# Kernel tuning notes

Hardware: AMD Instinct MI355X
Metric: run time of the kernel (lower is better)

## Reference

```python
import jax, jax.numpy as jnp
import numpy as np

D, H, DFF, NE, ND, B = 512, 8, 2048, 64, 64, 16

def _ln(x, g, b):
    m = x.mean(-1, keepdims=True)
    v = ((x - m) ** 2).mean(-1, keepdims=True)
    return (x - m) * jax.lax.rsqrt(v + 1e-5) * g + b

def _mha(q, k, v, Wi, bi, Wo, bo, h=H):
    # q,k,v: (L, B, d) seq-first, like torch nn.MultiheadAttention (eval mode)
    Lq, Bb, d = q.shape
    hd = d // h
    Wq, Wk, Wv = jnp.split(Wi, 3, axis=0)
    bq, bk, bv = jnp.split(bi, 3)
    def proj(x, W, bb):
        y = x @ W.T + bb                                  # (L, B, d)
        return y.reshape(x.shape[0], Bb, h, hd).transpose(1, 2, 0, 3)  # (B, h, L, hd)
    qh = proj(q, Wq, bq) * (hd ** -0.5)
    kh = proj(k, Wk, bk)
    vh = proj(v, Wv, bv)
    a = jax.nn.softmax(jnp.einsum('bhqe,bhke->bhqk', qh, kh), axis=-1)
    o = jnp.einsum('bhqk,bhke->bhqe', a, vh).transpose(2, 0, 1, 3).reshape(Lq, Bb, d)
    return o @ Wo.T + bo

def _ffn(x, W1, b1, W2, b2):
    return jax.nn.relu(x @ W1.T + b1) @ W2.T + b2

def _forward(enc, dec, ec_Wi, ec_bi, ec_Wo, ec_bo, dc_Wi, dc_bi, dc_Wo, dc_bo,
             es_Wi, es_bi, es_Wo, es_bo, ds_Wi, ds_bi, ds_Wo, ds_bo,
             eff_W1, eff_b1, eff_W2, eff_b2, dff_W1, dff_b1, dff_W2, dff_b2,
             n_ec_g, n_ec_b, n_es_g, n_es_b, n_ef_g, n_ef_b, n_dc_g, n_dc_b,
             n_dci_g, n_dci_b, n_ds_g, n_ds_b, n_df_g, n_df_b, pW, pWb, pv, pb):
    f_n = _ln(enc, n_ec_g, n_ec_b)   # (ne, B, d) -- normed once, reused for all j
    G_n = _ln(dec, n_dc_g, n_dc_b)   # (nd, B, d)
    # dec_cross for all j at once (key/value is the single token f_j)
    dc_out = jax.vmap(lambda fj: _mha(G_n, fj[None], fj[None], dc_Wi, dc_bi, dc_Wo, dc_bo))(f_n)  # (ne, nd, B, d)
    G_fj = dec[None] + dc_out                            # (ne, nd, B, d)
    G_im = _ln(G_fj, n_dci_g, n_dci_b)
    # enc_cross for all j at once (query is the single token f_j)
    ec_out = jax.vmap(lambda fj, Gj: _mha(fj[None], Gj, Gj, ec_Wi, ec_bi, ec_Wo, ec_bo)[0])(f_n, G_im)  # (ne, B, d)
    enc1 = enc + ec_out
    # attention pooling over the ne fusion copies
    G_c = G_fj.transpose(2, 1, 0, 3)                     # (B, nd, ne, d)
    energy = jnp.tanh(G_c @ pW.T + pWb + pb)
    w = jax.nn.softmax(energy @ pv.T, axis=2)            # (B, nd, ne, 1)
    dec1 = (G_c * w).sum(axis=2).transpose(1, 0, 2)      # (nd, B, d)
    # self-attention + FFN (pre-norm residual)
    en = _ln(enc1, n_es_g, n_es_b)
    enc2 = enc1 + _mha(en, en, en, es_Wi, es_bi, es_Wo, es_bo)
    dn = _ln(dec1, n_ds_g, n_ds_b)
    dec2 = dec1 + _mha(dn, dn, dn, ds_Wi, ds_bi, ds_Wo, ds_bo)
    enc3 = enc2 + _ffn(_ln(enc2, n_ef_g, n_ef_b), eff_W1, eff_b1, eff_W2, eff_b2)
    dec3 = dec2 + _ffn(_ln(dec2, n_df_g, n_df_b), dff_W1, dff_b1, dff_W2, dff_b2)
    return (enc3, dec3)

def setup_inputs() -> dict:
    key = jax.random.key(0)
    ks = iter(jax.random.split(key, 64))
    def w(shape, scale=0.05):
        return jax.random.normal(next(ks), shape, jnp.float32) * scale
    d, dff = D, DFF
    inp = {
        'enc': jax.random.normal(next(ks), (NE, B, d), jnp.float32),
        'dec': jax.random.normal(next(ks), (ND, B, d), jnp.float32),
    }
    for p in ['ec', 'dc', 'es', 'ds']:
        inp[p + '_Wi'] = w((3 * d, d)); inp[p + '_bi'] = jnp.zeros(3 * d, jnp.float32)
        inp[p + '_Wo'] = w((d, d)); inp[p + '_bo'] = jnp.zeros(d, jnp.float32)
    for p in ['eff', 'dff']:
        inp[p + '_W1'] = w((dff, d)); inp[p + '_b1'] = jnp.zeros(dff, jnp.float32)
        inp[p + '_W2'] = w((d, dff)); inp[p + '_b2'] = jnp.zeros(d, jnp.float32)
    for p in ['n_ec', 'n_es', 'n_ef', 'n_dc', 'n_dci', 'n_ds', 'n_df']:
        inp[p + '_g'] = jnp.ones(d, jnp.float32); inp[p + '_b'] = jnp.zeros(d, jnp.float32)
    inp['pW'] = w((d, d)); inp['pWb'] = jnp.zeros(d, jnp.float32)
    inp['pv'] = w((1, d)); inp['pb'] = jnp.zeros(d, jnp.float32)
    return inp

def reference(enc, dec, ec_Wi, ec_bi, ec_Wo, ec_bo, dc_Wi, dc_bi, dc_Wo, dc_bo,
              es_Wi, es_bi, es_Wo, es_bo, ds_Wi, ds_bi, ds_Wo, ds_bo,
              eff_W1, eff_b1, eff_W2, eff_b2, dff_W1, dff_b1, dff_W2, dff_b2,
              n_ec_g, n_ec_b, n_es_g, n_es_b, n_ef_g, n_ef_b, n_dc_g, n_dc_b,
              n_dci_g, n_dci_b, n_ds_g, n_ds_b, n_df_g, n_df_b, pW, pWb, pv, pb):
    return _forward(enc, dec, ec_Wi, ec_bi, ec_Wo, ec_bo, dc_Wi, dc_bi, dc_Wo, dc_bo,
                    es_Wi, es_bi, es_Wo, es_bo, ds_Wi, ds_bi, ds_Wo, ds_bo,
                    eff_W1, eff_b1, eff_W2, eff_b2, dff_W1, dff_b1, dff_W2, dff_b2,
                    n_ec_g, n_ec_b, n_es_g, n_es_b, n_ef_g, n_ef_b, n_dc_g, n_dc_b,
                    n_dci_g, n_dci_b, n_ds_g, n_ds_b, n_df_g, n_df_b, pW, pWb, pv, pb)
```

## Files before the change

kernel.cpp:

```cpp
#include <hip/hip_runtime.h>


typedef __bf16 bf16_t;
typedef bf16_t bf16x8 __attribute__((ext_vector_type(8)));
typedef float f32x4 __attribute__((ext_vector_type(4)));
typedef unsigned short u16x4 __attribute__((ext_vector_type(4)));
typedef unsigned short u16x8 __attribute__((ext_vector_type(8)));

__device__ inline unsigned short f2bf(float f) {
  unsigned int u = __float_as_uint(f);
  u += 0x7fffu + ((u >> 16) & 1u);
  return (unsigned short)(u >> 16);
}
__device__ inline float bf2f(unsigned short u) {
  return __uint_as_float(((unsigned int)u) << 16);
}

__device__ inline float wsum(float v) {
#pragma unroll
  for (int o = 1; o < 64; o <<= 1) v += __shfl_xor(v, o);
  return v;
}
__device__ inline float wmax(float v) {
#pragma unroll
  for (int o = 1; o < 64; o <<= 1) v = fmaxf(v, __shfl_xor(v, o));
  return v;
}

struct CastJob {
  const float* src;
  unsigned short* dst;
  int n;
  const float* cs;
};
struct CastBatch {
  CastJob j[15];
};

__global__ __launch_bounds__(256) void cast_w(CastBatch cb) {
  const CastJob jb = cb.j[blockIdx.y];
  const int stride = 32 * 256 * 4;
  for (int i = (blockIdx.x * 256 + threadIdx.x) * 4; i < jb.n; i += stride) {
    float4 v = *(const float4*)(jb.src + i);
    if (jb.cs) {
      int k = i & 511;
      v.x *= jb.cs[k];
      v.y *= jb.cs[k + 1];
      v.z *= jb.cs[k + 2];
      v.w *= jb.cs[k + 3];
    }
    u16x4 o = {f2bf(v.x), f2bf(v.y), f2bf(v.z), f2bf(v.w)};
    *(u16x4*)(jb.dst + i) = o;
  }
}

__device__ inline void ln_body(const float* __restrict__ x,
                               const float* __restrict__ g,
                               const float* __restrict__ be,
                               unsigned short* __restrict__ y, int t) {
  float v0 = x[t], v1 = x[t + 256];
  float s = wsum(v0 + v1);
  float s2 = wsum(v0 * v0 + v1 * v1);
  __shared__ float sh[8];
  int w = t >> 6, lane = t & 63;
  if (lane == 0) { sh[w] = s; sh[4 + w] = s2; }
  __syncthreads();
  s = sh[0] + sh[1] + sh[2] + sh[3];
  s2 = sh[4] + sh[5] + sh[6] + sh[7];
  float mean = s * (1.f / 512.f);
  float var = s2 * (1.f / 512.f) - mean * mean;
  float r = rsqrtf(var + 1e-5f);
  y[t] = f2bf((v0 - mean) * r * g[t] + be[t]);
  y[t + 256] = f2bf((v1 - mean) * r * g[t + 256] + be[t + 256]);
}

__device__ inline void stats_body(const float* __restrict__ x,
                                  float* __restrict__ m, float* __restrict__ q2,
                                  unsigned short* __restrict__ xb, int t,
                                  int row) {
  float v0 = x[t], v1 = x[t + 256];
  if (xb) {
    xb[t] = f2bf(v0);
    xb[t + 256] = f2bf(v1);
  }
  float s = wsum(v0 + v1);
  float s2 = wsum(v0 * v0 + v1 * v1);
  __shared__ float sh2[8];
  int w = t >> 6, lane = t & 63;
  if (lane == 0) { sh2[w] = s; sh2[4 + w] = s2; }
  __syncthreads();
  if (t == 0) {
    s = sh2[0] + sh2[1] + sh2[2] + sh2[3];
    s2 = sh2[4] + sh2[5] + sh2[6] + sh2[7];
    m[row] = s * (1.f / 512.f);
    q2[row] = s2 * (1.f / 512.f);
  }
}

__global__ __launch_bounds__(256) void ln_stats_kernel(
    const float* __restrict__ enc, const float* __restrict__ g,
    const float* __restrict__ be, unsigned short* __restrict__ f_n,
    const float* __restrict__ dec, float* __restrict__ md,
    float* __restrict__ q2d, unsigned short* __restrict__ dec_b) {
  int row = blockIdx.x;
  if (row < 1024) {
    ln_body(enc + (size_t)row * 512, g, be, f_n + (size_t)row * 512,
            threadIdx.x);
  } else {
    row -= 1024;
    stats_body(dec + (size_t)row * 512, md, q2d, dec_b + (size_t)row * 512,
               threadIdx.x, row);
  }
}

__global__ __launch_bounds__(256) void stats_kernel(
    const float* __restrict__ X, float* __restrict__ m, float* __restrict__ q2,
    unsigned short* __restrict__ Xb) {
  int row = blockIdx.x;
  stats_body(X + (size_t)row * 512, m, q2,
             Xb ? Xb + (size_t)row * 512 : nullptr, threadIdx.x, row);
}

__global__ __launch_bounds__(256) void ln2_kernel(
    const float* __restrict__ X0, const float* __restrict__ g0,
    const float* __restrict__ b0, unsigned short* __restrict__ Y0,
    const float* __restrict__ X1, const float* __restrict__ g1,
    const float* __restrict__ b1, unsigned short* __restrict__ Y1) {
  int row = blockIdx.x;
  if (row < 1024) {
    ln_body(X0 + (size_t)row * 512, g0, b0, Y0 + (size_t)row * 512, threadIdx.x);
  } else {
    row -= 1024;
    ln_body(X1 + (size_t)row * 512, g1, b1, Y1 + (size_t)row * 512, threadIdx.x);
  }
}

__global__ __launch_bounds__(256) void uvec_kernel(
    const float* __restrict__ Wk, const float* __restrict__ Wv,
    const float* __restrict__ bk, const float* __restrict__ bv,
    const float* __restrict__ g, const float* __restrict__ beta,
    float* __restrict__ u_k, float* __restrict__ u_v,
    float* __restrict__ c_k, float* __restrict__ c_v) {
  int n = blockIdx.x * 4 + (threadIdx.x >> 6);
  int lane = threadIdx.x & 63;
  const float* wk = Wk + (size_t)n * 512;
  const float* wv = Wv + (size_t)n * 512;
  float uk = 0.f, uv = 0.f, ck = 0.f, cv = 0.f;
#pragma unroll
  for (int k0 = 0; k0 < 512; k0 += 64) {
    int k = k0 + lane;
    float a = wk[k], b2 = wv[k], gg = g[k], bb = beta[k];
    uk += a * gg;
    ck += a * bb;
    uv += b2 * gg;
    cv += b2 * bb;
  }
  uk = wsum(uk);
  uv = wsum(uv);
  ck = wsum(ck);
  cv = wsum(cv);
  if (lane == 0) {
    u_k[n] = uk;
    u_v[n] = uv;
    c_k[n] = ck + bk[n];
    c_v[n] = cv + bv[n];
  }
}

__global__ __launch_bounds__(256) void mr_kernel(
    const unsigned short* __restrict__ decb, const unsigned short* __restrict__ tbb,
    const float* __restrict__ md, const float* __restrict__ q2d,
    const float* __restrict__ mt, const float* __restrict__ q2t,
    float* __restrict__ mArr, float* __restrict__ rArr) {
  int wid = blockIdx.x * 4 + (threadIdx.x >> 6);
  int lane = threadIdx.x & 63;
  int b = wid & 15;
  int i = (wid >> 4) & 63;
  int j = wid >> 10;
  const unsigned short* dr = decb + (size_t)(i * 16 + b) * 512 + lane * 8;
  const unsigned short* tr = tbb + (size_t)(j * 16 + b) * 512 + lane * 8;
  u16x8 a = *(const u16x8*)dr;
  u16x8 c = *(const u16x8*)tr;
  float s = 0.f;
#pragma unroll
  for (int k = 0; k < 8; ++k) s += bf2f(a[k]) * bf2f(c[k]);
  s = wsum(s);
  if (lane == 0) {
    float mean = md[i * 16 + b] + mt[j * 16 + b];
    float msq = q2d[i * 16 + b] + q2t[j * 16 + b] + 2.f * s * (1.f / 512.f);
    float var = msq - mean * mean;
    int idx = b * 4096 + j * 64 + i;
    mArr[idx] = mean;
    rArr[idx] = rsqrtf(var + 1e-5f);
  }
}

__global__ __launch_bounds__(256) void ec_attn(
    const unsigned short* __restrict__ Qe, const unsigned short* __restrict__ Kd,
    const unsigned short* __restrict__ Kt, const unsigned short* __restrict__ Vd,
    const unsigned short* __restrict__ Vt, const float* __restrict__ u_k,
    const float* __restrict__ u_v, const float* __restrict__ c_k,
    const float* __restrict__ c_v, const float* __restrict__ mArr,
    const float* __restrict__ rArr, unsigned short* __restrict__ O) {
  int h = blockIdx.x & 7;
  int b = blockIdx.x >> 3;
  __shared__ unsigned short Qs[64][72];
  __shared__ unsigned short Ks[64][72];
  __shared__ unsigned short VdT[64][72];
  __shared__ unsigned short Ps[64][72];
  __shared__ float ms[64][66];
  __shared__ float rs[64][66];
  __shared__ float stp[64][4], sup[64][4], scp[64][4];
  __shared__ float stv[64], suv[64], scv[64], swv[64], swmv[64];
  int t = threadIdx.x;
  {
    int row = t >> 2;
    int qt = t & 3;
    int cb = qt * 16;
    size_t base = (size_t)(row * 16 + b) * 512 + h * 64 + cb;
    u16x8 q0 = *(const u16x8*)(Qe + base);
    u16x8 q1 = *(const u16x8*)(Qe + base + 8);
    u16x8 k0 = *(const u16x8*)(Kd + base);
    u16x8 k1 = *(const u16x8*)(Kd + base + 8);
    u16x8 kt0 = *(const u16x8*)(Kt + base);
    u16x8 kt1 = *(const u16x8*)(Kt + base + 8);
    u16x8 v0 = *(const u16x8*)(Vd + base);
    u16x8 v1 = *(const u16x8*)(Vd + base + 8);
    *(u16x8*)&Qs[row][cb] = q0;
    *(u16x8*)&Qs[row][cb + 8] = q1;
    *(u16x8*)&Ks[row][cb] = k0;
    *(u16x8*)&Ks[row][cb + 8] = k1;
#pragma unroll
    for (int jj = 0; jj < 8; ++jj) VdT[cb + jj][row] = v0[jj];
#pragma unroll
    for (int jj = 0; jj < 8; ++jj) VdT[cb + 8 + jj][row] = v1[jj];
    float st_ = 0.f, su_ = 0.f, sc_ = 0.f;
#pragma unroll
    for (int jj = 0; jj < 8; ++jj) {
      float qa = bf2f(q0[jj]), qb = bf2f(q1[jj]);
      st_ += qa * bf2f(kt0[jj]) + qb * bf2f(kt1[jj]);
      su_ += qa * u_k[h * 64 + cb + jj] + qb * u_k[h * 64 + cb + 8 + jj];
      sc_ += qa * c_k[h * 64 + cb + jj] + qb * c_k[h * 64 + cb + 8 + jj];
    }
    stp[row][qt] = st_;
    sup[row][qt] = su_;
    scp[row][qt] = sc_;
  }
#pragma unroll
  for (int k = 0; k < 16; ++k) {
    int idx = t + k * 256;
    ms[idx >> 6][idx & 63] = mArr[(size_t)b * 4096 + idx];
    rs[idx >> 6][idx & 63] = rArr[(size_t)b * 4096 + idx];
  }
  __syncthreads();
  if (t < 64) {
    stv[t] = stp[t][0] + stp[t][1] + stp[t][2] + stp[t][3];
    suv[t] = sup[t][0] + sup[t][1] + sup[t][2] + sup[t][3];
    scv[t] = scp[t][0] + scp[t][1] + scp[t][2] + scp[t][3];
  }
  __syncthreads();
  int wave = t >> 6, lane = t & 63;
  int fr = lane & 15, fg = lane >> 4;
  f32x4 sacc[4] = {};
  bf16x8 aq0 = *(const bf16x8*)&Qs[wave * 16 + fr][fg * 8];
  bf16x8 aq1 = *(const bf16x8*)&Qs[wave * 16 + fr][32 + fg * 8];
#pragma unroll
  for (int nt = 0; nt < 4; ++nt) {
    bf16x8 b0 = *(const bf16x8*)&Ks[nt * 16 + fr][fg * 8];
    bf16x8 b1 = *(const bf16x8*)&Ks[nt * 16 + fr][32 + fg * 8];
    sacc[nt] = __builtin_amdgcn_mfma_f32_16x16x32_bf16(aq0, b0, sacc[nt], 0, 0, 0);
    sacc[nt] = __builtin_amdgcn_mfma_f32_16x16x32_bf16(aq1, b1, sacc[nt], 0, 0, 0);
  }
#pragma unroll
  for (int r = 0; r < 4; ++r) {
    int j = wave * 16 + fg * 4 + r;
    float stj = stv[j], suj = suv[j], scj = scv[j];
    float a0, a1, a2, a3;
    {
      int i0 = fr, i1 = 16 + fr, i2 = 32 + fr, i3 = 48 + fr;
      a0 = rs[j][i0] * (sacc[0][r] + stj - ms[j][i0] * suj) + scj;
      a1 = rs[j][i1] * (sacc[1][r] + stj - ms[j][i1] * suj) + scj;
      a2 = rs[j][i2] * (sacc[2][r] + stj - ms[j][i2] * suj) + scj;
      a3 = rs[j][i3] * (sacc[3][r] + stj - ms[j][i3] * suj) + scj;
    }
    float mx = fmaxf(fmaxf(a0, a1), fmaxf(a2, a3));
#pragma unroll
    for (int o = 1; o < 16; o <<= 1) mx = fmaxf(mx, __shfl_xor(mx, o));
    a0 = __expf(a0 - mx);
    a1 = __expf(a1 - mx);
    a2 = __expf(a2 - mx);
    a3 = __expf(a3 - mx);
    float se = a0 + a1 + a2 + a3;
#pragma unroll
    for (int o = 1; o < 16; o <<= 1) se += __shfl_xor(se, o);
    float inv = 1.f / se;
    float w0 = a0 * inv * rs[j][fr];
    float w1 = a1 * inv * rs[j][16 + fr];
    float w2 = a2 * inv * rs[j][32 + fr];
    float w3 = a3 * inv * rs[j][48 + fr];
    float sw = w0 + w1 + w2 + w3;
    float swm = w0 * ms[j][fr] + w1 * ms[j][16 + fr] + w2 * ms[j][32 + fr] +
                w3 * ms[j][48 + fr];
#pragma unroll
    for (int o = 1; o < 16; o <<= 1) {
      sw += __shfl_xor(sw, o);
      swm += __shfl_xor(swm, o);
    }
    Ps[j][fr] = f2bf(w0);
    Ps[j][16 + fr] = f2bf(w1);
    Ps[j][32 + fr] = f2bf(w2);
    Ps[j][48 + fr] = f2bf(w3);
    if (fr == 0) {
      swv[j] = sw;
      swmv[j] = swm;
    }
  }
  f32x4 oc[4] = {};
  bf16x8 ap0 = *(const bf16x8*)&Ps[wave * 16 + fr][fg * 8];
  bf16x8 ap1 = *(const bf16x8*)&Ps[wave * 16 + fr][32 + fg * 8];
#pragma unroll
  for (int nt = 0; nt < 4; ++nt) {
    bf16x8 b0 = *(const bf16x8*)&VdT[nt * 16 + fr][fg * 8];
    bf16x8 b1 = *(const bf16x8*)&VdT[nt * 16 + fr][32 + fg * 8];
    oc[nt] = __builtin_amdgcn_mfma_f32_16x16x32_bf16(ap0, b0, oc[nt], 0, 0, 0);
    oc[nt] = __builtin_amdgcn_mfma_f32_16x16x32_bf16(ap1, b1, oc[nt], 0, 0, 0);
  }
#pragma unroll
  for (int nt = 0; nt < 4; ++nt) {
    int d = nt * 16 + fr;
    float uvd = u_v[h * 64 + d];
    float cvd = c_v[h * 64 + d];
#pragma unroll
    for (int r = 0; r < 4; ++r) {
      int j = wave * 16 + fg * 4 + r;
      size_t gidx = (size_t)(j * 16 + b) * 512 + h * 64 + d;
      float o = oc[nt][r] + swv[j] * bf2f(Vt[gidx]) - swmv[j] * uvd + cvd;
      O[gidx] = f2bf(o);
    }
  }
}

__global__ __launch_bounds__(256) void pool_kernel(
    const float* __restrict__ Ed, const float* __restrict__ Et,
    const float* __restrict__ pv, const float* __restrict__ dec,
    const unsigned short* __restrict__ tbf, float* __restrict__ dec1) {
  int i = blockIdx.x;
  int b = blockIdx.y;
  int t = threadIdx.x;
  int wave = t >> 6, lane = t & 63;
  float edv[8], pvv[8];
  const float* ed = Ed + (size_t)(i * 16 + b) * 512;
#pragma unroll
  for (int c = 0; c < 8; ++c) {
    edv[c] = ed[c * 64 + lane];
    pvv[c] = pv[c * 64 + lane];
  }
  __shared__ float esh[64];
  __shared__ float wsh[64];
#pragma unroll 1
  for (int jl = 0; jl < 16; ++jl) {
    int j = wave * 16 + jl;
    const float* et = Et + (size_t)(j * 16 + b) * 512;
    float s = 0.f;
#pragma unroll
    for (int c = 0; c < 8; ++c) {
      float x = edv[c] + et[c * 64 + lane];
      float e2 = __expf(2.f * x);
      float th = 1.f - 2.f * __builtin_amdgcn_rcpf(e2 + 1.f);
      s += th * pvv[c];
    }
    s = wsum(s);
    if (lane == 0) esh[j] = s;
  }
  __syncthreads();
  if (t < 64) {
    float e = esh[t];
    float mx = wmax(e);
    float ex = __expf(e - mx);
    float se = wsum(ex);
    wsh[t] = ex / se;
  }
  __syncthreads();
  size_t rowib = (size_t)(i * 16 + b) * 512;
  int d2 = t * 2;
  float2 dv = *(const float2*)(dec + rowib + d2);
  float acc0 = dv.x, acc1 = dv.y;
#pragma unroll 8
  for (int j2 = 0; j2 < 64; ++j2) {
    const unsigned short* tp = tbf + (size_t)(j2 * 16 + b) * 512 + d2;
    float w = wsh[j2];
    acc0 += w * bf2f(tp[0]);
    acc1 += w * bf2f(tp[1]);
  }
  float2 ov = {acc0, acc1};
  *(float2*)(dec1 + rowib + d2) = ov;
}

__global__ __launch_bounds__(256) void self_attn(
    const unsigned short* __restrict__ QKVe, unsigned short* __restrict__ Oe,
    const unsigned short* __restrict__ QKVd, unsigned short* __restrict__ Od) {
  const unsigned short* QKV = blockIdx.y ? QKVd : QKVe;
  unsigned short* O = blockIdx.y ? Od : Oe;
  int h = blockIdx.x & 7;
  int b = blockIdx.x >> 3;
  __shared__ unsigned short Qs[64][72];
  __shared__ unsigned short Ksh[64][72];
  __shared__ unsigned short VT[64][72];
  __shared__ unsigned short Ps[64][72];
  int t = threadIdx.x;
  {
    int row = t >> 2;
    int cb = (t & 3) * 16;
    const unsigned short* src =
        QKV + (size_t)(row * 16 + b) * 1536 + h * 64 + cb;
    u16x8 q0 = *(const u16x8*)(src);
    u16x8 q1 = *(const u16x8*)(src + 8);
    u16x8 k0 = *(const u16x8*)(src + 512);
    u16x8 k1 = *(const u16x8*)(src + 520);
    u16x8 v0 = *(const u16x8*)(src + 1024);
    u16x8 v1 = *(const u16x8*)(src + 1032);
    *(u16x8*)&Qs[row][cb] = q0;
    *(u16x8*)&Qs[row][cb + 8] = q1;
    *(u16x8*)&Ksh[row][cb] = k0;
    *(u16x8*)&Ksh[row][cb + 8] = k1;
#pragma unroll
    for (int jj = 0; jj < 8; ++jj) VT[cb + jj][row] = v0[jj];
#pragma unroll
    for (int jj = 0; jj < 8; ++jj) VT[cb + 8 + jj][row] = v1[jj];
  }
  __syncthreads();
  int wave = t >> 6, lane = t & 63;
  int fr = lane & 15, fg = lane >> 4;
  f32x4 sc[4] = {};
  bf16x8 aq0 = *(const bf16x8*)&Qs[wave * 16 + fr][fg * 8];
  bf16x8 aq1 = *(const bf16x8*)&Qs[wave * 16 + fr][32 + fg * 8];
#pragma unroll
  for (int nt = 0; nt < 4; ++nt) {
    bf16x8 b0 = *(const bf16x8*)&Ksh[nt * 16 + fr][fg * 8];
    bf16x8 b1 = *(const bf16x8*)&Ksh[nt * 16 + fr][32 + fg * 8];
    sc[nt] = __builtin_amdgcn_mfma_f32_16x16x32_bf16(aq0, b0, sc[nt], 0, 0, 0);
    sc[nt] = __builtin_amdgcn_mfma_f32_16x16x32_bf16(aq1, b1, sc[nt], 0, 0, 0);
  }
#pragma unroll
  for (int r = 0; r < 4; ++r) {
    float a0 = sc[0][r] * 0.125f, a1 = sc[1][r] * 0.125f;
    float a2 = sc[2][r] * 0.125f, a3 = sc[3][r] * 0.125f;
    float mx = fmaxf(fmaxf(a0, a1), fmaxf(a2, a3));
#pragma unroll
    for (int o = 1; o < 16; o <<= 1) mx = fmaxf(mx, __shfl_xor(mx, o));
    a0 = __expf(a0 - mx);
    a1 = __expf(a1 - mx);
    a2 = __expf(a2 - mx);
    a3 = __expf(a3 - mx);
    float se = a0 + a1 + a2 + a3;
#pragma unroll
    for (int o = 1; o < 16; o <<= 1) se += __shfl_xor(se, o);
    float inv = 1.f / se;
    int prow = wave * 16 + fg * 4 + r;
    Ps[prow][0 + fr] = f2bf(a0 * inv);
    Ps[prow][16 + fr] = f2bf(a1 * inv);
    Ps[prow][32 + fr] = f2bf(a2 * inv);
    Ps[prow][48 + fr] = f2bf(a3 * inv);
  }
  f32x4 oc[4] = {};
  bf16x8 ap0 = *(const bf16x8*)&Ps[wave * 16 + fr][fg * 8];
  bf16x8 ap1 = *(const bf16x8*)&Ps[wave * 16 + fr][32 + fg * 8];
#pragma unroll
  for (int nt = 0; nt < 4; ++nt) {
    bf16x8 b0 = *(const bf16x8*)&VT[nt * 16 + fr][fg * 8];
    bf16x8 b1 = *(const bf16x8*)&VT[nt * 16 + fr][32 + fg * 8];
    oc[nt] = __builtin_amdgcn_mfma_f32_16x16x32_bf16(ap0, b0, oc[nt], 0, 0, 0);
    oc[nt] = __builtin_amdgcn_mfma_f32_16x16x32_bf16(ap1, b1, oc[nt], 0, 0, 0);
  }
#pragma unroll
  for (int nt = 0; nt < 4; ++nt) {
#pragma unroll
    for (int r = 0; r < 4; ++r) {
      int q = wave * 16 + fg * 4 + r;
      int d = nt * 16 + fr;
      O[(size_t)(q * 16 + b) * 512 + h * 64 + d] = f2bf(oc[nt][r]);
    }
  }
}

struct GemmJob {
  const unsigned short* X;
  const unsigned short* W;
  const float* bias;
  const float* resid;
  float* Y;
  unsigned short* Ybf;
  float scale;
  int relu;
};
struct GemmBatch {
  GemmJob j[5];
};

__global__ __launch_bounds__(256) void gemm_bf16(GemmBatch gb, int M, int N,
                                                 int K) {
  const GemmJob jb = gb.j[blockIdx.z];
  __shared__ unsigned short As[64][72];
  __shared__ unsigned short Bs[64][72];
  const int t = threadIdx.x;
  const int lane = t & 63;
  const int wave = t >> 6;
  const int wr = wave >> 1;
  const int wc = wave & 1;
  const int bm = blockIdx.y * 64;
  const int bn = blockIdx.x * 64;

  f32x4 acc[2][2] = {};
  const unsigned short* Xp = jb.X + (size_t)bm * K;
  const unsigned short* Wp = jb.W + (size_t)bn * K;

  const int c0 = t, c1 = t + 256;
  const int r0 = c0 >> 3, o0 = (c0 & 7) * 8;
  const int r1 = c1 >> 3, o1 = (c1 & 7) * 8;

  u16x8 xa0 = *(const u16x8*)&Xp[(size_t)r0 * K + o0];
  u16x8 xa1 = *(const u16x8*)&Xp[(size_t)r1 * K + o1];
  u16x8 wa0 = *(const u16x8*)&Wp[(size_t)r0 * K + o0];
  u16x8 wa1 = *(const u16x8*)&Wp[(size_t)r1 * K + o1];

  for (int k0 = 0; k0 < K; k0 += 64) {
    *(u16x8*)&As[r0][o0] = xa0;
    *(u16x8*)&As[r1][o1] = xa1;
    *(u16x8*)&Bs[r0][o0] = wa0;
    *(u16x8*)&Bs[r1][o1] = wa1;
    __syncthreads();
    if (k0 + 64 < K) {
      int kn = k0 + 64;
      xa0 = *(const u16x8*)&Xp[(size_t)r0 * K + kn + o0];
      xa1 = *(const u16x8*)&Xp[(size_t)r1 * K + kn + o1];
      wa0 = *(const u16x8*)&Wp[(size_t)r0 * K + kn + o0];
      wa1 = *(const u16x8*)&Wp[(size_t)r1 * K + kn + o1];
    }
#pragma unroll
    for (int ks = 0; ks < 2; ++ks) {
      int kk = ks * 32 + (lane >> 4) * 8;
      int fr = lane & 15;
      bf16x8 a0 = *(const bf16x8*)&As[wr * 32 + fr][kk];
      bf16x8 a1 = *(const bf16x8*)&As[wr * 32 + 16 + fr][kk];
      bf16x8 b0 = *(const bf16x8*)&Bs[wc * 32 + fr][kk];
      bf16x8 b1 = *(const bf16x8*)&Bs[wc * 32 + 16 + fr][kk];
      acc[0][0] = __builtin_amdgcn_mfma_f32_16x16x32_bf16(a0, b0, acc[0][0], 0, 0, 0);
      acc[0][1] = __builtin_amdgcn_mfma_f32_16x16x32_bf16(a0, b1, acc[0][1], 0, 0, 0);
      acc[1][0] = __builtin_amdgcn_mfma_f32_16x16x32_bf16(a1, b0, acc[1][0], 0, 0, 0);
      acc[1][1] = __builtin_amdgcn_mfma_f32_16x16x32_bf16(a1, b1, acc[1][1], 0, 0, 0);
    }
    __syncthreads();
  }
#pragma unroll
  for (int mt = 0; mt < 2; ++mt) {
#pragma unroll
    for (int nt = 0; nt < 2; ++nt) {
      int col = bn + wc * 32 + nt * 16 + (lane & 15);
      int rowb = bm + wr * 32 + mt * 16 + (lane >> 4) * 4;
      float bia = jb.bias ? jb.bias[col] : 0.f;
#pragma unroll
      for (int r = 0; r < 4; ++r) {
        float v = (acc[mt][nt][r] + bia) * jb.scale;
        if (jb.relu) v = fmaxf(v, 0.f);
        if (jb.resid) v += jb.resid[(size_t)(rowb + r) * N + col];
        size_t idx = (size_t)(rowb + r) * N + col;
        if (jb.Y) jb.Y[idx] = v;
        if (jb.Ybf) jb.Ybf[idx] = f2bf(v);
      }
    }
  }
}

extern "C" void kernel_launch(void* const* d_in, const int* in_sizes, int n_in,
                              void* d_out, int out_size, void* d_ws,
                              size_t ws_size, hipStream_t stream) {
  const float* enc = (const float*)d_in[0];
  const float* dec = (const float*)d_in[1];
  const float* ec_Wi = (const float*)d_in[2];
  const float* ec_bi = (const float*)d_in[3];
  const float* ec_Wo = (const float*)d_in[4];
  const float* ec_bo = (const float*)d_in[5];
  const float* dc_Wi = (const float*)d_in[6];
  const float* dc_bi = (const float*)d_in[7];
  const float* dc_Wo = (const float*)d_in[8];
  const float* dc_bo = (const float*)d_in[9];
  const float* es_Wi = (const float*)d_in[10];
  const float* es_bi = (const float*)d_in[11];
  const float* es_Wo = (const float*)d_in[12];
  const float* es_bo = (const float*)d_in[13];
  const float* ds_Wi = (const float*)d_in[14];
  const float* ds_bi = (const float*)d_in[15];
  const float* ds_Wo = (const float*)d_in[16];
  const float* ds_bo = (const float*)d_in[17];
  const float* eff_W1 = (const float*)d_in[18];
  const float* eff_b1 = (const float*)d_in[19];
  const float* eff_W2 = (const float*)d_in[20];
  const float* eff_b2 = (const float*)d_in[21];
  const float* dff_W1 = (const float*)d_in[22];
  const float* dff_b1 = (const float*)d_in[23];
  const float* dff_W2 = (const float*)d_in[24];
  const float* dff_b2 = (const float*)d_in[25];
  const float* n_ec_g = (const float*)d_in[26];
  const float* n_ec_b = (const float*)d_in[27];
  const float* n_es_g = (const float*)d_in[28];
  const float* n_es_b = (const float*)d_in[29];
  const float* n_ef_g = (const float*)d_in[30];
  const float* n_ef_b = (const float*)d_in[31];
  const float* n_dci_g = (const float*)d_in[34];
  const float* n_dci_b = (const float*)d_in[35];
  const float* n_ds_g = (const float*)d_in[36];
  const float* n_ds_b = (const float*)d_in[37];
  const float* n_df_g = (const float*)d_in[38];
  const float* n_df_b = (const float*)d_in[39];
  const float* pW = (const float*)d_in[40];
  const float* pWb = (const float*)d_in[41];
  const float* pv = (const float*)d_in[42];
  const float* pb = (const float*)d_in[43];

  float* ws = (float*)d_ws;
  const size_t U = 524288;
  float* Ed = ws + 3 * U;
  float* tb = ws + 4 * U;
  float* Et = ws + 7 * U;
  float* enc1 = ws + 8 * U;
  float* dec1 = ws + 9 * U;
  float* enc2 = ws + 10 * U;
  float* dec2 = ws + 11 * U;
  float* sm = ws + 12 * U;
  float* md = sm;
  float* q2d = sm + 1024;
  float* mt = sm + 2048;
  float* q2t = sm + 3072;
  float* u_k = sm + 4096;
  float* u_v = sm + 4608;
  float* c_k = sm + 5120;
  float* c_v = sm + 5632;
  float* mArr = sm + 6144;
  float* rArr = sm + 6144 + 65536;
  unsigned short* ub0 = (unsigned short*)ws;
  unsigned short* Qe_b = ub0 + 0 * U;
  unsigned short* Kd_b = ub0 + 1 * U;
  unsigned short* Vd_b = ub0 + 2 * U;
  unsigned short* Kt_b = ub0 + 3 * U;
  unsigned short* Vt_b = ub0 + 4 * U;
  unsigned short* ub = (unsigned short*)(ws + 12 * U + 137216);
  const int W262 = 262144, W786 = 786432, W1M = 1048576;
  unsigned short* w_dcWv = ub;
  unsigned short* w_ecWq = w_dcWv + W262;
  unsigned short* w_ecWkg = w_ecWq + W262;
  unsigned short* w_ecWvg = w_ecWkg + W262;
  unsigned short* w_pW = w_ecWvg + W262;
  unsigned short* w_dcWo = w_pW + W262;
  unsigned short* w_ecWo = w_dcWo + W262;
  unsigned short* w_esWi = w_ecWo + W262;
  unsigned short* w_dsWi = w_esWi + W786;
  unsigned short* w_esWo = w_dsWi + W786;
  unsigned short* w_dsWo = w_esWo + W262;
  unsigned short* w_effW1 = w_dsWo + W262;
  unsigned short* w_dffW1 = w_effW1 + W1M;
  unsigned short* w_effW2 = w_dffW1 + W1M;
  unsigned short* w_dffW2 = w_effW2 + W1M;
  unsigned short* actb = w_dffW2 + W1M;
  unsigned short* f_n_b = actb;
  unsigned short* V1_b = actb + U;
  unsigned short* dec_b = actb + 2 * U;
  unsigned short* tb_b = actb + 3 * U;
  unsigned short* Oec_b = actb + 4 * U;
  unsigned short* nbE = f_n_b;
  unsigned short* nbD = V1_b;
  unsigned short* OaE = dec_b;
  unsigned short* OaD = tb_b;
  unsigned short* QKVe_b = (unsigned short*)(ws + 0 * U);
  unsigned short* QKVd_b = (unsigned short*)(ws + 2 * U);
  unsigned short* He_b = (unsigned short*)(ws + 0 * U);
  unsigned short* Hd_b = (unsigned short*)(ws + 2 * U);

  const float* dc_Wv = dc_Wi + 1024 * 512;
  const float* dc_bv = dc_bi + 1024;
  const float* ec_Wq = ec_Wi;
  const float* ec_bq = ec_bi;
  const float* ec_Wk = ec_Wi + 512 * 512;
  const float* ec_bk = ec_bi + 512;
  const float* ec_Wv = ec_Wi + 1024 * 512;
  const float* ec_bv = ec_bi + 1024;

  {
    CastBatch cb{};
    cb.j[0] = {dc_Wv, w_dcWv, W262, nullptr};
    cb.j[1] = {ec_Wq, w_ecWq, W262, nullptr};
    cb.j[2] = {ec_Wk, w_ecWkg, W262, n_dci_g};
    cb.j[3] = {ec_Wv, w_ecWvg, W262, n_dci_g};
    cb.j[4] = {pW, w_pW, W262, nullptr};
    cb.j[5] = {dc_Wo, w_dcWo, W262, nullptr};
    cb.j[6] = {ec_Wo, w_ecWo, W262, nullptr};
    cb.j[7] = {es_Wi, w_esWi, W786, nullptr};
    cb.j[8] = {ds_Wi, w_dsWi, W786, nullptr};
    cb.j[9] = {es_Wo, w_esWo, W262, nullptr};
    cb.j[10] = {ds_Wo, w_dsWo, W262, nullptr};
    cb.j[11] = {eff_W1, w_effW1, W1M, nullptr};
    cb.j[12] = {dff_W1, w_dffW1, W1M, nullptr};
    cb.j[13] = {eff_W2, w_effW2, W1M, nullptr};
    cb.j[14] = {dff_W2, w_dffW2, W1M, nullptr};
    cast_w<<<dim3(32, 15), 256, 0, stream>>>(cb);
  }
  ln_stats_kernel<<<2048, 256, 0, stream>>>(enc, n_ec_g, n_ec_b, f_n_b, dec,
                                            md, q2d, dec_b);
  uvec_kernel<<<128, 256, 0, stream>>>(ec_Wk, ec_Wv, ec_bk, ec_bv, n_dci_g,
                                       n_dci_b, u_k, u_v, c_k, c_v);
  {
    GemmBatch gb{};
    gb.j[0] = {f_n_b, w_dcWv, dc_bv, nullptr, nullptr, V1_b, 1.f, 0};
    gb.j[1] = {f_n_b, w_ecWq, ec_bq, nullptr, nullptr, Qe_b, 0.125f, 0};
    gb.j[2] = {dec_b, w_ecWkg, nullptr, nullptr, nullptr, Kd_b, 1.f, 0};
    gb.j[3] = {dec_b, w_ecWvg, nullptr, nullptr, nullptr, Vd_b, 1.f, 0};
    gb.j[4] = {dec_b, w_pW, pWb, nullptr, Ed, nullptr, 1.f, 0};
    gemm_bf16<<<dim3(8, 16, 5), 256, 0, stream>>>(gb, 1024, 512, 512);
  }
  {
    GemmBatch gb{};
    gb.j[0] = {V1_b, w_dcWo, dc_bo, nullptr, tb, tb_b, 1.f, 0};
    gemm_bf16<<<dim3(8, 16, 1), 256, 0, stream>>>(gb, 1024, 512, 512);
  }
  stats_kernel<<<1024, 256, 0, stream>>>(tb, mt, q2t, nullptr);
  {
    GemmBatch gb{};
    gb.j[0] = {tb_b, w_ecWkg, nullptr, nullptr, nullptr, Kt_b, 1.f, 0};
    gb.j[1] = {tb_b, w_ecWvg, nullptr, nullptr, nullptr, Vt_b, 1.f, 0};
    gb.j[2] = {tb_b, w_pW, pb, nullptr, Et, nullptr, 1.f, 0};
    gemm_bf16<<<dim3(8, 16, 3), 256, 0, stream>>>(gb, 1024, 512, 512);
  }
  mr_kernel<<<16384, 256, 0, stream>>>(dec_b, tb_b, md, q2d, mt, q2t, mArr,
                                       rArr);
  ec_attn<<<128, 256, 0, stream>>>(Qe_b, Kd_b, Kt_b, Vd_b, Vt_b, u_k, u_v, c_k,
                                   c_v, mArr, rArr, Oec_b);
  pool_kernel<<<dim3(64, 16), 256, 0, stream>>>(Ed, Et, pv, dec, tb_b, dec1);
  {
    GemmBatch gb{};
    gb.j[0] = {Oec_b, w_ecWo, ec_bo, enc, enc1, nullptr, 1.f, 0};
    gemm_bf16<<<dim3(8, 16, 1), 256, 0, stream>>>(gb, 1024, 512, 512);
  }
  ln2_kernel<<<2048, 256, 0, stream>>>(enc1, n_es_g, n_es_b, nbE, dec1, n_ds_g,
                                       n_ds_b, nbD);
  {
    GemmBatch gb{};
    gb.j[0] = {nbE, w_esWi, es_bi, nullptr, nullptr, QKVe_b, 1.f, 0};
    gb.j[1] = {nbD, w_dsWi, ds_bi, nullptr, nullptr, QKVd_b, 1.f, 0};
    gemm_bf16<<<dim3(24, 16, 2), 256, 0, stream>>>(gb, 1024, 1536, 512);
  }
  self_attn<<<dim3(128, 2), 256, 0, stream>>>(QKVe_b, OaE, QKVd_b, OaD);
  {
    GemmBatch gb{};
    gb.j[0] = {OaE, w_esWo, es_bo, enc1, enc2, nullptr, 1.f, 0};
    gb.j[1] = {OaD, w_dsWo, ds_bo, dec1, dec2, nullptr, 1.f, 0};
    gemm_bf16<<<dim3(8, 16, 2), 256, 0, stream>>>(gb, 1024, 512, 512);
  }
  ln2_kernel<<<2048, 256, 0, stream>>>(enc2, n_ef_g, n_ef_b, nbE, dec2, n_df_g,
                                       n_df_b, nbD);
  {
    GemmBatch gb{};
    gb.j[0] = {nbE, w_effW1, eff_b1, nullptr, nullptr, He_b, 1.f, 1};
    gb.j[1] = {nbD, w_dffW1, dff_b1, nullptr, nullptr, Hd_b, 1.f, 1};
    gemm_bf16<<<dim3(32, 16, 2), 256, 0, stream>>>(gb, 1024, 2048, 512);
  }
  float* out = (float*)d_out;
  {
    GemmBatch gb{};
    gb.j[0] = {He_b, w_effW2, eff_b2, enc2, out, nullptr, 1.f, 0};
    gb.j[1] = {Hd_b, w_dffW2, dff_b2, dec2, out + U, nullptr, 1.f, 0};
    gemm_bf16<<<dim3(8, 16, 2), 256, 0, stream>>>(gb, 1024, 512, 2048);
  }
}
```

Before: 317.8 us.

## Fuse LayerNorms into GEMMs, merge casts/stats/uvec and mr into fewer launches

Removes the standalone LayerNorm, stats, uvec, mr and cast kernels. GEMM epilogues now accumulate per-row sum and sum-of-squares with atomics, and the following GEMM applies LayerNorm while loading its fp32 input tile. Weight casts are spread between a merged phase0 kernel and an extra z-slice of the first GEMM. The mr dot products run as an MFMA slice of another GEMM, and ec_attn and pool are merged into one attnpool kernel that also produces dec1 stats. This cuts launch count and intermediate traffic, but adds atomics, per-tile recomputation of normalization, and variance computed as E[x^2]-mean^2.

Result: slower. 339.8 us (+6.9%).

```diff
diff --git a/kernel.cpp b/kernel.cpp
--- a/kernel.cpp
+++ b/kernel.cpp
@@ -33,26 +33,6 @@
   int n;
   const float* cs;
 };
-struct CastBatch {
-  CastJob j[15];
-};
-
-__global__ __launch_bounds__(256) void cast_w(CastBatch cb) {
-  const CastJob jb = cb.j[blockIdx.y];
-  const int stride = 32 * 256 * 4;
-  for (int i = (blockIdx.x * 256 + threadIdx.x) * 4; i < jb.n; i += stride) {
-    float4 v = *(const float4*)(jb.src + i);
-    if (jb.cs) {
-      int k = i & 511;
-      v.x *= jb.cs[k];
-      v.y *= jb.cs[k + 1];
-      v.z *= jb.cs[k + 2];
-      v.w *= jb.cs[k + 3];
-    }
-    u16x4 o = {f2bf(v.x), f2bf(v.y), f2bf(v.z), f2bf(v.w)};
-    *(u16x4*)(jb.dst + i) = o;
-  }
-}
 
 __device__ inline void ln_body(const float* __restrict__ x,
                                const float* __restrict__ g,
@@ -97,113 +77,327 @@
   }
 }
 
-__global__ __launch_bounds__(256) void ln_stats_kernel(
-    const float* __restrict__ enc, const float* __restrict__ g,
-    const float* __restrict__ be, unsigned short* __restrict__ f_n,
-    const float* __restrict__ dec, float* __restrict__ md,
-    float* __restrict__ q2d, unsigned short* __restrict__ dec_b) {
-  int row = blockIdx.x;
-  if (row < 1024) {
-    ln_body(enc + (size_t)row * 512, g, be, f_n + (size_t)row * 512,
-            threadIdx.x);
+struct Phase0Args {
+  const float* enc; const float* g_ec; const float* b_ec; unsigned short* f_n;
+  const float* dec; float* md; float* q2d; unsigned short* dec_b;
+  CastJob cast[6];
+  const float* Wk; const float* Wv; const float* bk; const float* bv;
+  const float* g_dci; const float* b_dci;
+  float* u_k; float* u_v; float* c_k; float* c_v;
+  float* zbase; int zcount;
+};
+
+__global__ __launch_bounds__(256) void phase0(Phase0Args a) {
+  int bx = blockIdx.x;
+  const int t = threadIdx.x;
+  if (bx < 2048) {
+    int row = bx;
+    if (row < 1024) {
+      ln_body(a.enc + (size_t)row * 512, a.g_ec, a.b_ec,
+              a.f_n + (size_t)row * 512, t);
+    } else {
+      row -= 1024;
+      stats_body(a.dec + (size_t)row * 512, a.md, a.q2d,
+                 a.dec_b + (size_t)row * 512, t, row);
+    }
+    return;
+  }
+  bx -= 2048;
+  if (bx < 256) {
+    const int total = 6 * 262144;
+    const int stride = 256 * 256 * 4;
+    for (int e = (bx * 256 + t) * 4; e < total; e += stride) {
+      int jj = e >> 18;
+      int i = e & 262143;
+      const CastJob cj = a.cast[jj];
+      float4 v = *(const float4*)(cj.src + i);
+      if (cj.cs) {
+        int k = i & 511;
+        v.x *= cj.cs[k]; v.y *= cj.cs[k + 1];
+        v.z *= cj.cs[k + 2]; v.w *= cj.cs[k + 3];
+      }
+      u16x4 o = {f2bf(v.x), f2bf(v.y), f2bf(v.z), f2bf(v.w)};
+      *(u16x4*)(cj.dst + i) = o;
+    }
+    return;
+  }
+  bx -= 256;
+  if (bx < 128) {
+    int n = bx * 4 + (t >> 6);
+    int lane = t & 63;
+    const float* wk = a.Wk + (size_t)n * 512;
+    const float* wv = a.Wv + (size_t)n * 512;
+    float uk = 0.f, uv = 0.f, ck = 0.f, cv = 0.f;
+#pragma unroll
+    for (int k0 = 0; k0 < 512; k0 += 64) {
+      int k = k0 + lane;
+      float x = wk[k], y = wv[k], gg = a.g_dci[k], bb = a.b_dci[k];
+      uk += x * gg; ck += x * bb;
+      uv += y * gg; cv += y * bb;
+    }
+    uk = wsum(uk); uv = wsum(uv); ck = wsum(ck); cv = wsum(cv);
+    if (lane == 0) {
+      a.u_k[n] = uk; a.u_v[n] = uv;
+      a.c_k[n] = ck + a.bk[n]; a.c_v[n] = cv + a.bv[n];
+    }
+    return;
+  }
+  for (int i = t; i < a.zcount; i += 256) a.zbase[i] = 0.f;
+}
+
+struct GemmJob {
+  const unsigned short* X;
+  const float* Xf;
+  const float* Asum; const float* Asq;
+  const float* g; const float* be;
+  const unsigned short* W;
+  const float* bias;
+  const float* resid;
+  float* Y;
+  unsigned short* Ybf;
+  float* Ssum; float* Ssq;
+  float scale;
+  int relu;
+};
+struct MrJob {
+  const unsigned short* A; const unsigned short* B;
+  const float* md; const float* q2d;
+  const float* ts; const float* tsq;
+  float* mArr; float* rArr;
+};
+struct GemmBatch {
+  GemmJob j[5];
+  MrJob mr;
+  CastJob c[9];
+};
+
+__device__ inline u16x8 fold_pack(float4 va, float4 vb, const float* gp,
+                                  const float* bp, float m, float ri) {
+  float4 g0 = *(const float4*)gp;
+  float4 g1 = *(const float4*)(gp + 4);
+  float4 e0 = *(const float4*)bp;
+  float4 e1 = *(const float4*)(bp + 4);
+  u16x8 o;
+  o[0] = f2bf((va.x - m) * ri * g0.x + e0.x);
+  o[1] = f2bf((va.y - m) * ri * g0.y + e0.y);
+  o[2] = f2bf((va.z - m) * ri * g0.z + e0.z);
+  o[3] = f2bf((va.w - m) * ri * g0.w + e0.w);
+  o[4] = f2bf((vb.x - m) * ri * g1.x + e1.x);
+  o[5] = f2bf((vb.y - m) * ri * g1.y + e1.y);
+  o[6] = f2bf((vb.z - m) * ri * g1.z + e1.z);
+  o[7] = f2bf((vb.w - m) * ri * g1.w + e1.w);
+  return o;
+}
+
+__global__ __launch_bounds__(256) void gemm_bf16(GemmBatch gb, int M, int N,
+                                                 int K, int cast_z, int mr_z) {
+  const int t = threadIdx.x;
+  if ((int)blockIdx.z == cast_z) {
+    const int nb = gridDim.x * gridDim.y;
+    const int bid = blockIdx.y * gridDim.x + blockIdx.x;
+    const int stride = nb * 256 * 4;
+#pragma unroll 1
+    for (int jj = 0; jj < 9; ++jj) {
+      const CastJob cj = gb.c[jj];
+      if (!cj.src) continue;
+      for (int i = (bid * 256 + t) * 4; i < cj.n; i += stride) {
+        float4 v = *(const float4*)(cj.src + i);
+        u16x4 o = {f2bf(v.x), f2bf(v.y), f2bf(v.z), f2bf(v.w)};
+        *(u16x4*)(cj.dst + i) = o;
+      }
+    }
+    return;
+  }
+  __shared__ unsigned short As[64][72];
+  __shared__ unsigned short Bs[64][72];
+  const int lane = t & 63;
+  const int wave = t >> 6;
+  const int wr = wave >> 1;
+  const int wc = wave & 1;
+  const int fr = lane & 15;
+  const int fg = lane >> 4;
+  const int c1 = t + 256;
+  const int r0 = t >> 3, o0 = (t & 7) * 8;
+  const int r1 = c1 >> 3, o1 = (c1 & 7) * 8;
+
+  if ((int)blockIdx.z == mr_z) {
+    const int bb = blockIdx.y * gridDim.x + blockIdx.x;
+    if (bb >= 16) return;
+    const unsigned short* Ap = gb.mr.A + (size_t)bb * 512;
+    const unsigned short* Bp = gb.mr.B + (size_t)bb * 512;
+    f32x4 acc[2][2] = {};
+    for (int k0 = 0; k0 < 512; k0 += 64) {
+      *(u16x8*)&As[r0][o0] = *(const u16x8*)&Ap[(size_t)r0 * 8192 + k0 + o0];
+      *(u16x8*)&As[r1][o1] = *(const u16x8*)&Ap[(size_t)r1 * 8192 + k0 + o1];
+      *(u16x8*)&Bs[r0][o0] = *(const u16x8*)&Bp[(size_t)r0 * 8192 + k0 + o0];
+      *(u16x8*)&Bs[r1][o1] = *(const u16x8*)&Bp[(size_t)r1 * 8192 + k0 + o1];
+      __syncthreads();
+#pragma unroll
+      for (int ks = 0; ks < 2; ++ks) {
+        int kk = ks * 32 + fg * 8;
+        bf16x8 a0 = *(const bf16x8*)&As[wr * 32 + fr][kk];
+        bf16x8 a1 = *(const bf16x8*)&As[wr * 32 + 16 + fr][kk];
+        bf16x8 b0 = *(const bf16x8*)&Bs[wc * 32 + fr][kk];
+        bf16x8 b1 = *(const bf16x8*)&Bs[wc * 32 + 16 + fr][kk];
+        acc[0][0] = __builtin_amdgcn_mfma_f32_16x16x32_bf16(a0, b0, acc[0][0], 0, 0, 0);
+        acc[0][1] = __builtin_amdgcn_mfma_f32_16x16x32_bf16(a0, b1, acc[0][1], 0, 0, 0);
+        acc[1][0] = __builtin_amdgcn_mfma_f32_16x16x32_bf16(a1, b0, acc[1][0], 0, 0, 0);
+        acc[1][1] = __builtin_amdgcn_mfma_f32_16x16x32_bf16(a1, b1, acc[1][1], 0, 0, 0);
+      }
+      __syncthreads();
+    }
+#pragma unroll
+    for (int nt = 0; nt < 2; ++nt) {
+      int j = wc * 32 + nt * 16 + fr;
+      float mtv = gb.mr.ts[j * 16 + bb] * (1.f / 512.f);
+      float qtv = gb.mr.tsq[j * 16 + bb] * (1.f / 512.f);
+#pragma unroll
+      for (int mt = 0; mt < 2; ++mt) {
+        int ibase = wr * 32 + mt * 16 + fg * 4;
+#pragma unroll
+        for (int r = 0; r < 4; ++r) {
+          int i = ibase + r;
+          float s = acc[mt][nt][r];
+          float mean = gb.mr.md[i * 16 + bb] + mtv;
+          float msq = gb.mr.q2d[i * 16 + bb] + qtv + s * (2.f / 512.f);
+          int idx = bb * 4096 + j * 64 + i;
+          gb.mr.mArr[idx] = mean;
+          gb.mr.rArr[idx] = rsqrtf(msq - mean * mean + 1e-5f);
+        }
+      }
+    }
+    return;
+  }
+
+  const GemmJob jb = gb.j[blockIdx.z];
+  const int bm = blockIdx.y * 64;
+  const int bn = blockIdx.x * 64;
+  const bool fold = jb.Xf != nullptr;
+  f32x4 acc[2][2] = {};
+  const unsigned short* Wp = jb.W + (size_t)bn * K;
+  const unsigned short* Xp = jb.X ? jb.X + (size_t)bm * K : nullptr;
+
+  float lm0 = 0.f, lr0i = 0.f, lm1 = 0.f, lr1i = 0.f;
+  if (fold) {
+    float s = jb.Asum[bm + r0], q = jb.Asq[bm + r0];
+    lm0 = s * (1.f / 512.f);
+    lr0i = rsqrtf(q * (1.f / 512.f) - lm0 * lm0 + 1e-5f);
+    s = jb.Asum[bm + r1]; q = jb.Asq[bm + r1];
+    lm1 = s * (1.f / 512.f);
+    lr1i = rsqrtf(q * (1.f / 512.f) - lm1 * lm1 + 1e-5f);
+  }
+
+  u16x8 xa0, xa1;
+  float4 fa0a, fa0b, fa1a, fa1b;
+  if (fold) {
+    const float* p0 = jb.Xf + (size_t)(bm + r0) * K + o0;
+    const float* p1 = jb.Xf + (size_t)(bm + r1) * K + o1;
+    fa0a = *(const float4*)p0; fa0b = *(const float4*)(p0 + 4);
+    fa1a = *(const float4*)p1; fa1b = *(const float4*)(p1 + 4);
   } else {
-    row -= 1024;
-    stats_body(dec + (size_t)row * 512, md, q2d, dec_b + (size_t)row * 512,
-               threadIdx.x, row);
-  }
-}
-
-__global__ __launch_bounds__(256) void stats_kernel(
-    const float* __restrict__ X, float* __restrict__ m, float* __restrict__ q2,
-    unsigned short* __restrict__ Xb) {
-  int row = blockIdx.x;
-  stats_body(X + (size_t)row * 512, m, q2,
-             Xb ? Xb + (size_t)row * 512 : nullptr, threadIdx.x, row);
-}
-
-__global__ __launch_bounds__(256) void ln2_kernel(
-    const float* __restrict__ X0, const float* __restrict__ g0,
-    const float* __restrict__ b0, unsigned short* __restrict__ Y0,
-    const float* __restrict__ X1, const float* __restrict__ g1,
-    const float* __restrict__ b1, unsigned short* __restrict__ Y1) {
-  int row = blockIdx.x;
-  if (row < 1024) {
-    ln_body(X0 + (size_t)row * 512, g0, b0, Y0 + (size_t)row * 512, threadIdx.x);
-  } else {
-    row -= 1024;
-    ln_body(X1 + (size_t)row * 512, g1, b1, Y1 + (size_t)row * 512, threadIdx.x);
-  }
-}
-
-__global__ __launch_bounds__(256) void uvec_kernel(
-    const float* __restrict__ Wk, const float* __restrict__ Wv,
-    const float* __restrict__ bk, const float* __restrict__ bv,
-    const float* __restrict__ g, const float* __restrict__ beta,
-    float* __restrict__ u_k, float* __restrict__ u_v,
-    float* __restrict__ c_k, float* __restrict__ c_v) {
-  int n = blockIdx.x * 4 + (threadIdx.x >> 6);
-  int lane = threadIdx.x & 63;
-  const float* wk = Wk + (size_t)n * 512;
-  const float* wv = Wv + (size_t)n * 512;
-  float uk = 0.f, uv = 0.f, ck = 0.f, cv = 0.f;
-#pragma unroll
-  for (int k0 = 0; k0 < 512; k0 += 64) {
-    int k = k0 + lane;
-    float a = wk[k], b2 = wv[k], gg = g[k], bb = beta[k];
-    uk += a * gg;
-    ck += a * bb;
-    uv += b2 * gg;
-    cv += b2 * bb;
-  }
-  uk = wsum(uk);
-  uv = wsum(uv);
-  ck = wsum(ck);
-  cv = wsum(cv);
-  if (lane == 0) {
-    u_k[n] = uk;
-    u_v[n] = uv;
-    c_k[n] = ck + bk[n];
-    c_v[n] = cv + bv[n];
-  }
-}
-
-__global__ __launch_bounds__(256) void mr_kernel(
-    const unsigned short* __restrict__ decb, const unsigned short* __restrict__ tbb,
-    const float* __restrict__ md, const float* __restrict__ q2d,
-    const float* __restrict__ mt, const float* __restrict__ q2t,
-    float* __restrict__ mArr, float* __restrict__ rArr) {
-  int wid = blockIdx.x * 4 + (threadIdx.x >> 6);
-  int lane = threadIdx.x & 63;
-  int b = wid & 15;
-  int i = (wid >> 4) & 63;
-  int j = wid >> 10;
-  const unsigned short* dr = decb + (size_t)(i * 16 + b) * 512 + lane * 8;
-  const unsigned short* tr = tbb + (size_t)(j * 16 + b) * 512 + lane * 8;
-  u16x8 a = *(const u16x8*)dr;
-  u16x8 c = *(const u16x8*)tr;
-  float s = 0.f;
-#pragma unroll
-  for (int k = 0; k < 8; ++k) s += bf2f(a[k]) * bf2f(c[k]);
-  s = wsum(s);
-  if (lane == 0) {
-    float mean = md[i * 16 + b] + mt[j * 16 + b];
-    float msq = q2d[i * 16 + b] + q2t[j * 16 + b] + 2.f * s * (1.f / 512.f);
-    float var = msq - mean * mean;
-    int idx = b * 4096 + j * 64 + i;
-    mArr[idx] = mean;
-    rArr[idx] = rsqrtf(var + 1e-5f);
-  }
-}
-
-__global__ __launch_bounds__(256) void ec_attn(
+    xa0 = *(const u16x8*)&Xp[(size_t)r0 * K + o0];
+    xa1 = *(const u16x8*)&Xp[(size_t)r1 * K + o1];
+  }
+  u16x8 wa0 = *(const u16x8*)&Wp[(size_t)r0 * K + o0];
+  u16x8 wa1 = *(const u16x8*)&Wp[(size_t)r1 * K + o1];
+
+  for (int k0 = 0; k0 < K; k0 += 64) {
+    if (fold) {
+      *(u16x8*)&As[r0][o0] = fold_pack(fa0a, fa0b, jb.g + k0 + o0, jb.be + k0 + o0, lm0, lr0i);
+      *(u16x8*)&As[r1][o1] = fold_pack(fa1a, fa1b, jb.g + k0 + o1, jb.be + k0 + o1, lm1, lr1i);
+    } else {
+      *(u16x8*)&As[r0][o0] = xa0;
+      *(u16x8*)&As[r1][o1] = xa1;
+    }
+    *(u16x8*)&Bs[r0][o0] = wa0;
+    *(u16x8*)&Bs[r1][o1] = wa1;
+    __syncthreads();
+    if (k0 + 64 < K) {
+      const int kn = k0 + 64;
+      if (fold) {
+        const float* p0 = jb.Xf + (size_t)(bm + r0) * K + kn + o0;
+        const float* p1 = jb.Xf + (size_t)(bm + r1) * K + kn + o1;
+        fa0a = *(const float4*)p0; fa0b = *(const float4*)(p0 + 4);
+        fa1a = *(const float4*)p1; fa1b = *(const float4*)(p1 + 4);
+      } else {
+        xa0 = *(const u16x8*)&Xp[(size_t)r0 * K + kn + o0];
+        xa1 = *(const u16x8*)&Xp[(size_t)r1 * K + kn + o1];
+      }
+      wa0 = *(const u16x8*)&Wp[(size_t)r0 * K + kn + o0];
+      wa1 = *(const u16x8*)&Wp[(size_t)r1 * K + kn + o1];
+    }
+#pragma unroll
+    for (int ks = 0; ks < 2; ++ks) {
+      int kk = ks * 32 + fg * 8;
+      bf16x8 a0 = *(const bf16x8*)&As[wr * 32 + fr][kk];
+      bf16x8 a1 = *(const bf16x8*)&As[wr * 32 + 16 + fr][kk];
+      bf16x8 b0 = *(const bf16x8*)&Bs[wc * 32 + fr][kk];
+      bf16x8 b1 = *(const bf16x8*)&Bs[wc * 32 + 16 + fr][kk];
+      acc[0][0] = __builtin_amdgcn_mfma_f32_16x16x32_bf16(a0, b0, acc[0][0], 0, 0, 0);
+      acc[0][1] = __builtin_amdgcn_mfma_f32_16x16x32_bf16(a0, b1, acc[0][1], 0, 0, 0);
+      acc[1][0] = __builtin_amdgcn_mfma_f32_16x16x32_bf16(a1, b0, acc[1][0], 0, 0, 0);
+      acc[1][1] = __builtin_amdgcn_mfma_f32_16x16x32_bf16(a1, b1, acc[1][1], 0, 0, 0);
+    }
+    __syncthreads();
+  }
+  float rsum[2][4], rsq[2][4];
+  const bool dostat = jb.Ssum != nullptr;
+  if (dostat) {
+#pragma unroll
+    for (int mt = 0; mt < 2; ++mt)
+#pragma unroll
+      for (int r = 0; r < 4; ++r) { rsum[mt][r] = 0.f; rsq[mt][r] = 0.f; }
+  }
+#pragma unroll
+  for (int mt = 0; mt < 2; ++mt) {
+#pragma unroll
+    for (int nt = 0; nt < 2; ++nt) {
+      int col = bn + wc * 32 + nt * 16 + fr;
+      int rowb = bm + wr * 32 + mt * 16 + fg * 4;
+      float bia = jb.bias ? jb.bias[col] : 0.f;
+#pragma unroll
+      for (int r = 0; r < 4; ++r) {
+        float v = (acc[mt][nt][r] + bia) * jb.scale;
+        if (jb.relu) v = fmaxf(v, 0.f);
+        if (jb.resid) v += jb.resid[(size_t)(rowb + r) * N + col];
+        size_t idx = (size_t)(rowb + r) * N + col;
+        if (jb.Y) jb.Y[idx] = v;
+        if (jb.Ybf) jb.Ybf[idx] = f2bf(v);
+        if (dostat) { rsum[mt][r] += v; rsq[mt][r] += v * v; }
+      }
+    }
+  }
+  if (dostat) {
+#pragma unroll
+    for (int mt = 0; mt < 2; ++mt)
+#pragma unroll
+      for (int r = 0; r < 4; ++r) {
+        float s = rsum[mt][r], q = rsq[mt][r];
+#pragma unroll
+        for (int o = 1; o < 16; o <<= 1) {
+          s += __shfl_xor(s, o);
+          q += __shfl_xor(q, o);
+        }
+        if (fr == 0) {
+          int row = bm + wr * 32 + mt * 16 + fg * 4 + r;
+          atomicAdd(&jb.Ssum[row], s);
+          atomicAdd(&jb.Ssq[row], q);
+        }
+      }
+  }
+}
+
+__global__ __launch_bounds__(256) void attnpool(
     const unsigned short* __restrict__ Qe, const unsigned short* __restrict__ Kd,
     const unsigned short* __restrict__ Kt, const unsigned short* __restrict__ Vd,
     const unsigned short* __restrict__ Vt, const float* __restrict__ u_k,
     const float* __restrict__ u_v, const float* __restrict__ c_k,
     const float* __restrict__ c_v, const float* __restrict__ mArr,
-    const float* __restrict__ rArr, unsigned short* __restrict__ O) {
-  int h = blockIdx.x & 7;
-  int b = blockIdx.x >> 3;
+    const float* __restrict__ rArr, unsigned short* __restrict__ O,
+    const float* __restrict__ Ed, const float* __restrict__ Et,
+    const float* __restrict__ pv, const float* __restrict__ dec,
+    const unsigned short* __restrict__ tbf, float* __restrict__ dec1,
+    float* __restrict__ d1s, float* __restrict__ d1q) {
   __shared__ unsigned short Qs[64][72];
   __shared__ unsigned short Ks[64][72];
   __shared__ unsigned short VdT[64][72];
@@ -212,141 +406,141 @@
   __shared__ float rs[64][66];
   __shared__ float stp[64][4], sup[64][4], scp[64][4];
   __shared__ float stv[64], suv[64], scv[64], swv[64], swmv[64];
-  int t = threadIdx.x;
-  {
-    int row = t >> 2;
-    int qt = t & 3;
-    int cb = qt * 16;
-    size_t base = (size_t)(row * 16 + b) * 512 + h * 64 + cb;
-    u16x8 q0 = *(const u16x8*)(Qe + base);
-    u16x8 q1 = *(const u16x8*)(Qe + base + 8);
-    u16x8 k0 = *(const u16x8*)(Kd + base);
-    u16x8 k1 = *(const u16x8*)(Kd + base + 8);
-    u16x8 kt0 = *(const u16x8*)(Kt + base);
-    u16x8 kt1 = *(const u16x8*)(Kt + base + 8);
-    u16x8 v0 = *(const u16x8*)(Vd + base);
-    u16x8 v1 = *(const u16x8*)(Vd + base + 8);
-    *(u16x8*)&Qs[row][cb] = q0;
-    *(u16x8*)&Qs[row][cb + 8] = q1;
-    *(u16x8*)&Ks[row][cb] = k0;
-    *(u16x8*)&Ks[row][cb + 8] = k1;
-#pragma unroll
-    for (int jj = 0; jj < 8; ++jj) VdT[cb + jj][row] = v0[jj];
-#pragma unroll
-    for (int jj = 0; jj < 8; ++jj) VdT[cb + 8 + jj][row] = v1[jj];
-    float st_ = 0.f, su_ = 0.f, sc_ = 0.f;
-#pragma unroll
-    for (int jj = 0; jj < 8; ++jj) {
-      float qa = bf2f(q0[jj]), qb = bf2f(q1[jj]);
-      st_ += qa * bf2f(kt0[jj]) + qb * bf2f(kt1[jj]);
-      su_ += qa * u_k[h * 64 + cb + jj] + qb * u_k[h * 64 + cb + 8 + jj];
-      sc_ += qa * c_k[h * 64 + cb + jj] + qb * c_k[h * 64 + cb + 8 + jj];
-    }
-    stp[row][qt] = st_;
-    sup[row][qt] = su_;
-    scp[row][qt] = sc_;
-  }
-#pragma unroll
-  for (int k = 0; k < 16; ++k) {
-    int idx = t + k * 256;
-    ms[idx >> 6][idx & 63] = mArr[(size_t)b * 4096 + idx];
-    rs[idx >> 6][idx & 63] = rArr[(size_t)b * 4096 + idx];
-  }
-  __syncthreads();
-  if (t < 64) {
-    stv[t] = stp[t][0] + stp[t][1] + stp[t][2] + stp[t][3];
-    suv[t] = sup[t][0] + sup[t][1] + sup[t][2] + sup[t][3];
-    scv[t] = scp[t][0] + scp[t][1] + scp[t][2] + scp[t][3];
-  }
-  __syncthreads();
-  int wave = t >> 6, lane = t & 63;
-  int fr = lane & 15, fg = lane >> 4;
-  f32x4 sacc[4] = {};
-  bf16x8 aq0 = *(const bf16x8*)&Qs[wave * 16 + fr][fg * 8];
-  bf16x8 aq1 = *(const bf16x8*)&Qs[wave * 16 + fr][32 + fg * 8];
-#pragma unroll
-  for (int nt = 0; nt < 4; ++nt) {
-    bf16x8 b0 = *(const bf16x8*)&Ks[nt * 16 + fr][fg * 8];
-    bf16x8 b1 = *(const bf16x8*)&Ks[nt * 16 + fr][32 + fg * 8];
-    sacc[nt] = __builtin_amdgcn_mfma_f32_16x16x32_bf16(aq0, b0, sacc[nt], 0, 0, 0);
-    sacc[nt] = __builtin_amdgcn_mfma_f32_16x16x32_bf16(aq1, b1, sacc[nt], 0, 0, 0);
-  }
-#pragma unroll
-  for (int r = 0; r < 4; ++r) {
-    int j = wave * 16 + fg * 4 + r;
-    float stj = stv[j], suj = suv[j], scj = scv[j];
-    float a0, a1, a2, a3;
+  __shared__ float esh[64], wsh[64], pps[8];
+  const int t = threadIdx.x;
+  if (blockIdx.x < 128) {
+    int h = blockIdx.x & 7;
+    int b = blockIdx.x >> 3;
     {
-      int i0 = fr, i1 = 16 + fr, i2 = 32 + fr, i3 = 48 + fr;
-      a0 = rs[j][i0] * (sacc[0][r] + stj - ms[j][i0] * suj) + scj;
-      a1 = rs[j][i1] * (sacc[1][r] + stj - ms[j][i1] * suj) + scj;
-      a2 = rs[j][i2] * (sacc[2][r] + stj - ms[j][i2] * suj) + scj;
-      a3 = rs[j][i3] * (sacc[3][r] + stj - ms[j][i3] * suj) + scj;
-    }
-    float mx = fmaxf(fmaxf(a0, a1), fmaxf(a2, a3));
-#pragma unroll
-    for (int o = 1; o < 16; o <<= 1) mx = fmaxf(mx, __shfl_xor(mx, o));
-    a0 = __expf(a0 - mx);
-    a1 = __expf(a1 - mx);
-    a2 = __expf(a2 - mx);
-    a3 = __expf(a3 - mx);
-    float se = a0 + a1 + a2 + a3;
-#pragma unroll
-    for (int o = 1; o < 16; o <<= 1) se += __shfl_xor(se, o);
-    float inv = 1.f / se;
-    float w0 = a0 * inv * rs[j][fr];
-    float w1 = a1 * inv * rs[j][16 + fr];
-    float w2 = a2 * inv * rs[j][32 + fr];
-    float w3 = a3 * inv * rs[j][48 + fr];
-    float sw = w0 + w1 + w2 + w3;
-    float swm = w0 * ms[j][fr] + w1 * ms[j][16 + fr] + w2 * ms[j][32 + fr] +
-                w3 * ms[j][48 + fr];
-#pragma unroll
-    for (int o = 1; o < 16; o <<= 1) {
-      sw += __shfl_xor(sw, o);
-      swm += __shfl_xor(swm, o);
-    }
-    Ps[j][fr] = f2bf(w0);
-    Ps[j][16 + fr] = f2bf(w1);
-    Ps[j][32 + fr] = f2bf(w2);
-    Ps[j][48 + fr] = f2bf(w3);
-    if (fr == 0) {
-      swv[j] = sw;
-      swmv[j] = swm;
-    }
-  }
-  f32x4 oc[4] = {};
-  bf16x8 ap0 = *(const bf16x8*)&Ps[wave * 16 + fr][fg * 8];
-  bf16x8 ap1 = *(const bf16x8*)&Ps[wave * 16 + fr][32 + fg * 8];
-#pragma unroll
-  for (int nt = 0; nt < 4; ++nt) {
-    bf16x8 b0 = *(const bf16x8*)&VdT[nt * 16 + fr][fg * 8];
-    bf16x8 b1 = *(const bf16x8*)&VdT[nt * 16 + fr][32 + fg * 8];
-    oc[nt] = __builtin_amdgcn_mfma_f32_16x16x32_bf16(ap0, b0, oc[nt], 0, 0, 0);
-    oc[nt] = __builtin_amdgcn_mfma_f32_16x16x32_bf16(ap1, b1, oc[nt], 0, 0, 0);
-  }
-#pragma unroll
-  for (int nt = 0; nt < 4; ++nt) {
-    int d = nt * 16 + fr;
-    float uvd = u_v[h * 64 + d];
-    float cvd = c_v[h * 64 + d];
+      int row = t >> 2;
+      int qt = t & 3;
+      int cb = qt * 16;
+      size_t base = (size_t)(row * 16 + b) * 512 + h * 64 + cb;
+      u16x8 q0 = *(const u16x8*)(Qe + base);
+      u16x8 q1 = *(const u16x8*)(Qe + base + 8);
+      u16x8 k0 = *(const u16x8*)(Kd + base);
+      u16x8 k1 = *(const u16x8*)(Kd + base + 8);
+      u16x8 kt0 = *(const u16x8*)(Kt + base);
+      u16x8 kt1 = *(const u16x8*)(Kt + base + 8);
+      u16x8 v0 = *(const u16x8*)(Vd + base);
+      u16x8 v1 = *(const u16x8*)(Vd + base + 8);
+      *(u16x8*)&Qs[row][cb] = q0;
+      *(u16x8*)&Qs[row][cb + 8] = q1;
+      *(u16x8*)&Ks[row][cb] = k0;
+      *(u16x8*)&Ks[row][cb + 8] = k1;
+#pragma unroll
+      for (int jj = 0; jj < 8; ++jj) VdT[cb + jj][row] = v0[jj];
+#pragma unroll
+      for (int jj = 0; jj < 8; ++jj) VdT[cb + 8 + jj][row] = v1[jj];
+      float st_ = 0.f, su_ = 0.f, sc_ = 0.f;
+#pragma unroll
+      for (int jj = 0; jj < 8; ++jj) {
+        float qa = bf2f(q0[jj]), qb = bf2f(q1[jj]);
+        st_ += qa * bf2f(kt0[jj]) + qb * bf2f(kt1[jj]);
+        su_ += qa * u_k[h * 64 + cb + jj] + qb * u_k[h * 64 + cb + 8 + jj];
+        sc_ += qa * c_k[h * 64 + cb + jj] + qb * c_k[h * 64 + cb + 8 + jj];
+      }
+      stp[row][qt] = st_;
+      sup[row][qt] = su_;
+      scp[row][qt] = sc_;
+    }
+#pragma unroll
+    for (int k = 0; k < 16; ++k) {
+      int idx = t + k * 256;
+      ms[idx >> 6][idx & 63] = mArr[(size_t)b * 4096 + idx];
+      rs[idx >> 6][idx & 63] = rArr[(size_t)b * 4096 + idx];
+    }
+    __syncthreads();
+    if (t < 64) {
+      stv[t] = stp[t][0] + stp[t][1] + stp[t][2] + stp[t][3];
+      suv[t] = sup[t][0] + sup[t][1] + sup[t][2] + sup[t][3];
+      scv[t] = scp[t][0] + scp[t][1] + scp[t][2] + scp[t][3];
+    }
+    __syncthreads();
+    int wave = t >> 6, lane = t & 63;
+    int fr = lane & 15, fg = lane >> 4;
+    f32x4 sacc[4] = {};
+    bf16x8 aq0 = *(const bf16x8*)&Qs[wave * 16 + fr][fg * 8];
+    bf16x8 aq1 = *(const bf16x8*)&Qs[wave * 16 + fr][32 + fg * 8];
+#pragma unroll
+    for (int nt = 0; nt < 4; ++nt) {
+      bf16x8 b0 = *(const bf16x8*)&Ks[nt * 16 + fr][fg * 8];
+      bf16x8 b1 = *(const bf16x8*)&Ks[nt * 16 + fr][32 + fg * 8];
+      sacc[nt] = __builtin_amdgcn_mfma_f32_16x16x32_bf16(aq0, b0, sacc[nt], 0, 0, 0);
+      sacc[nt] = __builtin_amdgcn_mfma_f32_16x16x32_bf16(aq1, b1, sacc[nt], 0, 0, 0);
+    }
 #pragma unroll
     for (int r = 0; r < 4; ++r) {
       int j = wave * 16 + fg * 4 + r;
-      size_t gidx = (size_t)(j * 16 + b) * 512 + h * 64 + d;
-      float o = oc[nt][r] + swv[j] * bf2f(Vt[gidx]) - swmv[j] * uvd + cvd;
-      O[gidx] = f2bf(o);
-    }
-  }
-}
-
-__global__ __launch_bounds__(256) void pool_kernel(
-    const float* __restrict__ Ed, const float* __restrict__ Et,
-    const float* __restrict__ pv, const float* __restrict__ dec,
-    const unsigned short* __restrict__ tbf, float* __restrict__ dec1) {
-  int i = blockIdx.x;
-  int b = blockIdx.y;
-  int t = threadIdx.x;
+      float stj = stv[j], suj = suv[j], scj = scv[j];
+      float a0, a1, a2, a3;
+      {
+        int i0 = fr, i1 = 16 + fr, i2 = 32 + fr, i3 = 48 + fr;
+        a0 = rs[j][i0] * (sacc[0][r] + stj - ms[j][i0] * suj) + scj;
+        a1 = rs[j][i1] * (sacc[1][r] + stj - ms[j][i1] * suj) + scj;
+        a2 = rs[j][i2] * (sacc[2][r] + stj - ms[j][i2] * suj) + scj;
+        a3 = rs[j][i3] * (sacc[3][r] + stj - ms[j][i3] * suj) + scj;
+      }
+      float mx = fmaxf(fmaxf(a0, a1), fmaxf(a2, a3));
+#pragma unroll
+      for (int o = 1; o < 16; o <<= 1) mx = fmaxf(mx, __shfl_xor(mx, o));
+      a0 = __expf(a0 - mx);
+      a1 = __expf(a1 - mx);
+      a2 = __expf(a2 - mx);
+      a3 = __expf(a3 - mx);
+      float se = a0 + a1 + a2 + a3;
+#pragma unroll
+      for (int o = 1; o < 16; o <<= 1) se += __shfl_xor(se, o);
+      float inv = 1.f / se;
+      float w0 = a0 * inv * rs[j][fr];
+      float w1 = a1 * inv * rs[j][16 + fr];
+      float w2 = a2 * inv * rs[j][32 + fr];
+      float w3 = a3 * inv * rs[j][48 + fr];
+      float sw = w0 + w1 + w2 + w3;
+      float swm = w0 * ms[j][fr] + w1 * ms[j][16 + fr] + w2 * ms[j][32 + fr] +
+                  w3 * ms[j][48 + fr];
+#pragma unroll
+      for (int o = 1; o < 16; o <<= 1) {
+        sw += __shfl_xor(sw, o);
+        swm += __shfl_xor(swm, o);
+      }
+      Ps[j][fr] = f2bf(w0);
+      Ps[j][16 + fr] = f2bf(w1);
+      Ps[j][32 + fr] = f2bf(w2);
+      Ps[j][48 + fr] = f2bf(w3);
+      if (fr == 0) {
+        swv[j] = sw;
+        swmv[j] = swm;
+      }
+    }
+    f32x4 oc[4] = {};
+    bf16x8 ap0 = *(const bf16x8*)&Ps[wave * 16 + fr][fg * 8];
+    bf16x8 ap1 = *(const bf16x8*)&Ps[wave * 16 + fr][32 + fg * 8];
+#pragma unroll
+    for (int nt = 0; nt < 4; ++nt) {
+      bf16x8 b0 = *(const bf16x8*)&VdT[nt * 16 + fr][fg * 8];
+      bf16x8 b1 = *(const bf16x8*)&VdT[nt * 16 + fr][32 + fg * 8];
+      oc[nt] = __builtin_amdgcn_mfma_f32_16x16x32_bf16(ap0, b0, oc[nt], 0, 0, 0);
+      oc[nt] = __builtin_amdgcn_mfma_f32_16x16x32_bf16(ap1, b1, oc[nt], 0, 0, 0);
+    }
+#pragma unroll
+    for (int nt = 0; nt < 4; ++nt) {
+      int d = nt * 16 + fr;
+      float uvd = u_v[h * 64 + d];
+      float cvd = c_v[h * 64 + d];
+#pragma unroll
+      for (int r = 0; r < 4; ++r) {
+        int j = wave * 16 + fg * 4 + r;
+        size_t gidx = (size_t)(j * 16 + b) * 512 + h * 64 + d;
+        float o = oc[nt][r] + swv[j] * bf2f(Vt[gidx]) - swmv[j] * uvd + cvd;
+        O[gidx] = f2bf(o);
+      }
+    }
+    return;
+  }
+  int idx = blockIdx.x - 128;
+  int i = idx & 63;
+  int b = idx >> 6;
   int wave = t >> 6, lane = t & 63;
   float edv[8], pvv[8];
   const float* ed = Ed + (size_t)(i * 16 + b) * 512;
@@ -355,8 +549,6 @@
     edv[c] = ed[c * 64 + lane];
     pvv[c] = pv[c * 64 + lane];
   }
-  __shared__ float esh[64];
-  __shared__ float wsh[64];
 #pragma unroll 1
   for (int jl = 0; jl < 16; ++jl) {
     int j = wave * 16 + jl;
@@ -394,6 +586,16 @@
   }
   float2 ov = {acc0, acc1};
   *(float2*)(dec1 + rowib + d2) = ov;
+  float s1 = acc0 + acc1;
+  float s2v = acc0 * acc0 + acc1 * acc1;
+  s1 = wsum(s1);
+  s2v = wsum(s2v);
+  if (lane == 0) { pps[wave] = s1; pps[4 + wave] = s2v; }
+  __syncthreads();
+  if (t == 0) {
+    d1s[i * 16 + b] = pps[0] + pps[1] + pps[2] + pps[3];
+    d1q[i * 16 + b] = pps[4] + pps[5] + pps[6] + pps[7];
+  }
 }
 
 __global__ __launch_bounds__(256) void self_attn(
@@ -479,94 +681,6 @@
       int q = wave * 16 + fg * 4 + r;
       int d = nt * 16 + fr;
       O[(size_t)(q * 16 + b) * 512 + h * 64 + d] = f2bf(oc[nt][r]);
-    }
-  }
-}
-
-struct GemmJob {
-  const unsigned short* X;
-  const unsigned short* W;
-  const float* bias;
-  const float* resid;
-  float* Y;
-  unsigned short* Ybf;
-  float scale;
-  int relu;
-};
-struct GemmBatch {
-  GemmJob j[5];
-};
-
-__global__ __launch_bounds__(256) void gemm_bf16(GemmBatch gb, int M, int N,
-                                                 int K) {
-  const GemmJob jb = gb.j[blockIdx.z];
-  __shared__ unsigned short As[64][72];
-  __shared__ unsigned short Bs[64][72];
-  const int t = threadIdx.x;
-  const int lane = t & 63;
-  const int wave = t >> 6;
-  const int wr = wave >> 1;
-  const int wc = wave & 1;
-  const int bm = blockIdx.y * 64;
-  const int bn = blockIdx.x * 64;
-
-  f32x4 acc[2][2] = {};
-  const unsigned short* Xp = jb.X + (size_t)bm * K;
-  const unsigned short* Wp = jb.W + (size_t)bn * K;
-
-  const int c0 = t, c1 = t + 256;
-  const int r0 = c0 >> 3, o0 = (c0 & 7) * 8;
-  const int r1 = c1 >> 3, o1 = (c1 & 7) * 8;
-
-  u16x8 xa0 = *(const u16x8*)&Xp[(size_t)r0 * K + o0];
-  u16x8 xa1 = *(const u16x8*)&Xp[(size_t)r1 * K + o1];
-  u16x8 wa0 = *(const u16x8*)&Wp[(size_t)r0 * K + o0];
-  u16x8 wa1 = *(const u16x8*)&Wp[(size_t)r1 * K + o1];
-
-  for (int k0 = 0; k0 < K; k0 += 64) {
-    *(u16x8*)&As[r0][o0] = xa0;
-    *(u16x8*)&As[r1][o1] = xa1;
-    *(u16x8*)&Bs[r0][o0] = wa0;
-    *(u16x8*)&Bs[r1][o1] = wa1;
-    __syncthreads();
-    if (k0 + 64 < K) {
-      int kn = k0 + 64;
-      xa0 = *(const u16x8*)&Xp[(size_t)r0 * K + kn + o0];
-      xa1 = *(const u16x8*)&Xp[(size_t)r1 * K + kn + o1];
-      wa0 = *(const u16x8*)&Wp[(size_t)r0 * K + kn + o0];
-      wa1 = *(const u16x8*)&Wp[(size_t)r1 * K + kn + o1];
-    }
-#pragma unroll
-    for (int ks = 0; ks < 2; ++ks) {
-      int kk = ks * 32 + (lane >> 4) * 8;
-      int fr = lane & 15;
-      bf16x8 a0 = *(const bf16x8*)&As[wr * 32 + fr][kk];
-      bf16x8 a1 = *(const bf16x8*)&As[wr * 32 + 16 + fr][kk];
-      bf16x8 b0 = *(const bf16x8*)&Bs[wc * 32 + fr][kk];
-      bf16x8 b1 = *(const bf16x8*)&Bs[wc * 32 + 16 + fr][kk];
-      acc[0][0] = __builtin_amdgcn_mfma_f32_16x16x32_bf16(a0, b0, acc[0][0], 0, 0, 0);
-      acc[0][1] = __builtin_amdgcn_mfma_f32_16x16x32_bf16(a0, b1, acc[0][1], 0, 0, 0);
-      acc[1][0] = __builtin_amdgcn_mfma_f32_16x16x32_bf16(a1, b0, acc[1][0], 0, 0, 0);
-      acc[1][1] = __builtin_amdgcn_mfma_f32_16x16x32_bf16(a1, b1, acc[1][1], 0, 0, 0);
-    }
-    __syncthreads();
-  }
-#pragma unroll
-  for (int mt = 0; mt < 2; ++mt) {
-#pragma unroll
-    for (int nt = 0; nt < 2; ++nt) {
-      int col = bn + wc * 32 + nt * 16 + (lane & 15);
-      int rowb = bm + wr * 32 + mt * 16 + (lane >> 4) * 4;
-      float bia = jb.bias ? jb.bias[col] : 0.f;
-#pragma unroll
-      for (int r = 0; r < 4; ++r) {
-        float v = (acc[mt][nt][r] + bia) * jb.scale;
-        if (jb.relu) v = fmaxf(v, 0.f);
-        if (jb.resid) v += jb.resid[(size_t)(rowb + r) * N + col];
-        size_t idx = (size_t)(rowb + r) * N + col;
-        if (jb.Y) jb.Y[idx] = v;
-        if (jb.Ybf) jb.Ybf[idx] = f2bf(v);
-      }
     }
   }
 }
@@ -620,7 +734,6 @@
   float* ws = (float*)d_ws;
   const size_t U = 524288;
   float* Ed = ws + 3 * U;
-  float* tb = ws + 4 * U;
   float* Et = ws + 7 * U;
   float* enc1 = ws + 8 * U;
   float* dec1 = ws + 9 * U;
@@ -629,14 +742,23 @@
   float* sm = ws + 12 * U;
   float* md = sm;
   float* q2d = sm + 1024;
-  float* mt = sm + 2048;
-  float* q2t = sm + 3072;
   float* u_k = sm + 4096;
   float* u_v = sm + 4608;
   float* c_k = sm + 5120;
   float* c_v = sm + 5632;
   float* mArr = sm + 6144;
   float* rArr = sm + 6144 + 65536;
+  float* stx = ws + 24 * U;
+  float* t_s = stx;
+  float* t_sq = stx + 1024;
+  float* e1s = stx + 2048;
+  float* e1q = stx + 3072;
+  float* d1s = stx + 4096;
+  float* d1q = stx + 5120;
+  float* e2s = stx + 6144;
+  float* e2q = stx + 7168;
+  float* d2s = stx + 8192;
+  float* d2q = stx + 9216;
   unsigned short* ub0 = (unsigned short*)ws;
   unsigned short* Qe_b = ub0 + 0 * U;
   unsigned short* Kd_b = ub0 + 1 * U;
@@ -666,8 +788,6 @@
   unsigned short* dec_b = actb + 2 * U;
   unsigned short* tb_b = actb + 3 * U;
   unsigned short* Oec_b = actb + 4 * U;
-  unsigned short* nbE = f_n_b;
-  unsigned short* nbD = V1_b;
   unsigned short* OaE = dec_b;
   unsigned short* OaD = tb_b;
   unsigned short* QKVe_b = (unsigned short*)(ws + 0 * U);
@@ -684,89 +804,106 @@
   const float* ec_Wv = ec_Wi + 1024 * 512;
   const float* ec_bv = ec_bi + 1024;
 
+  auto J = [](const unsigned short* X, const unsigned short* W,
+              const float* bias, const float* resid, float* Y,
+              unsigned short* Ybf, float scale, int relu) {
+    GemmJob j{};
+    j.X = X; j.W = W; j.bias = bias; j.resid = resid;
+    j.Y = Y; j.Ybf = Ybf; j.scale = scale; j.relu = relu;
+    return j;
+  };
+  auto JF = [](const float* Xf, const float* As, const float* Aq,
+               const float* g, const float* be, const unsigned short* W,
+               const float* bias, unsigned short* Ybf, int relu) {
+    GemmJob j{};
+    j.Xf = Xf; j.Asum = As; j.Asq = Aq; j.g = g; j.be = be;
+    j.W = W; j.bias = bias; j.Ybf = Ybf; j.scale = 1.f; j.relu = relu;
+    return j;
+  };
+
   {
-    CastBatch cb{};
-    cb.j[0] = {dc_Wv, w_dcWv, W262, nullptr};
-    cb.j[1] = {ec_Wq, w_ecWq, W262, nullptr};
-    cb.j[2] = {ec_Wk, w_ecWkg, W262, n_dci_g};
-    cb.j[3] = {ec_Wv, w_ecWvg, W262, n_dci_g};
-    cb.j[4] = {pW, w_pW, W262, nullptr};
-    cb.j[5] = {dc_Wo, w_dcWo, W262, nullptr};
-    cb.j[6] = {ec_Wo, w_ecWo, W262, nullptr};
-    cb.j[7] = {es_Wi, w_esWi, W786, nullptr};
-    cb.j[8] = {ds_Wi, w_dsWi, W786, nullptr};
-    cb.j[9] = {es_Wo, w_esWo, W262, nullptr};
-    cb.j[10] = {ds_Wo, w_dsWo, W262, nullptr};
-    cb.j[11] = {eff_W1, w_effW1, W1M, nullptr};
-    cb.j[12] = {dff_W1, w_dffW1, W1M, nullptr};
-    cb.j[13] = {eff_W2, w_effW2, W1M, nullptr};
-    cb.j[14] = {dff_W2, w_dffW2, W1M, nullptr};
-    cast_w<<<dim3(32, 15), 256, 0, stream>>>(cb);
-  }
-  ln_stats_kernel<<<2048, 256, 0, stream>>>(enc, n_ec_g, n_ec_b, f_n_b, dec,
-                                            md, q2d, dec_b);
-  uvec_kernel<<<128, 256, 0, stream>>>(ec_Wk, ec_Wv, ec_bk, ec_bv, n_dci_g,
-                                       n_dci_b, u_k, u_v, c_k, c_v);
+    Phase0Args pa{};
+    pa.enc = enc; pa.g_ec = n_ec_g; pa.b_ec = n_ec_b; pa.f_n = f_n_b;
+    pa.dec = dec; pa.md = md; pa.q2d = q2d; pa.dec_b = dec_b;
+    pa.cast[0] = {dc_Wv, w_dcWv, W262, nullptr};
+    pa.cast[1] = {ec_Wq, w_ecWq, W262, nullptr};
+    pa.cast[2] = {ec_Wk, w_ecWkg, W262, n_dci_g};
+    pa.cast[3] = {ec_Wv, w_ecWvg, W262, n_dci_g};
+    pa.cast[4] = {pW, w_pW, W262, nullptr};
+    pa.cast[5] = {dc_Wo, w_dcWo, W262, nullptr};
+    pa.Wk = ec_Wk; pa.Wv = ec_Wv; pa.bk = ec_bk; pa.bv = ec_bv;
+    pa.g_dci = n_dci_g; pa.b_dci = n_dci_b;
+    pa.u_k = u_k; pa.u_v = u_v; pa.c_k = c_k; pa.c_v = c_v;
+    pa.zbase = stx; pa.zcount = 10240;
+    phase0<<<2433, 256, 0, stream>>>(pa);
+  }
   {
     GemmBatch gb{};
-    gb.j[0] = {f_n_b, w_dcWv, dc_bv, nullptr, nullptr, V1_b, 1.f, 0};
-    gb.j[1] = {f_n_b, w_ecWq, ec_bq, nullptr, nullptr, Qe_b, 0.125f, 0};
-    gb.j[2] = {dec_b, w_ecWkg, nullptr, nullptr, nullptr, Kd_b, 1.f, 0};
-    gb.j[3] = {dec_b, w_ecWvg, nullptr, nullptr, nullptr, Vd_b, 1.f, 0};
-    gb.j[4] = {dec_b, w_pW, pWb, nullptr, Ed, nullptr, 1.f, 0};
-    gemm_bf16<<<dim3(8, 16, 5), 256, 0, stream>>>(gb, 1024, 512, 512);
+    gb.j[0] = J(f_n_b, w_dcWv, dc_bv, nullptr, nullptr, V1_b, 1.f, 0);
+    gb.j[1] = J(f_n_b, w_ecWq, ec_bq, nullptr, nullptr, Qe_b, 0.125f, 0);
+    gb.j[2] = J(dec_b, w_ecWkg, nullptr, nullptr, nullptr, Kd_b, 1.f, 0);
+    gb.j[3] = J(dec_b, w_ecWvg, nullptr, nullptr, nullptr, Vd_b, 1.f, 0);
+    gb.j[4] = J(dec_b, w_pW, pWb, nullptr, Ed, nullptr, 1.f, 0);
+    gb.c[0] = {ec_Wo, w_ecWo, W262, nullptr};
+    gb.c[1] = {es_Wi, w_esWi, W786, nullptr};
+    gb.c[2] = {ds_Wi, w_dsWi, W786, nullptr};
+    gb.c[3] = {es_Wo, w_esWo, W262, nullptr};
+    gb.c[4] = {ds_Wo, w_dsWo, W262, nullptr};
+    gb.c[5] = {eff_W1, w_effW1, W1M, nullptr};
+    gb.c[6] = {dff_W1, w_dffW1, W1M, nullptr};
+    gb.c[7] = {eff_W2, w_effW2, W1M, nullptr};
+    gb.c[8] = {dff_W2, w_dffW2, W1M, nullptr};
+    gemm_bf16<<<dim3(8, 16, 6), 256, 0, stream>>>(gb, 1024, 512, 512, 5, -1);
   }
   {
     GemmBatch gb{};
-    gb.j[0] = {V1_b, w_dcWo, dc_bo, nullptr, tb, tb_b, 1.f, 0};
-    gemm_bf16<<<dim3(8, 16, 1), 256, 0, stream>>>(gb, 1024, 512, 512);
-  }
-  stats_kernel<<<1024, 256, 0, stream>>>(tb, mt, q2t, nullptr);
+    gb.j[0] = J(V1_b, w_dcWo, dc_bo, nullptr, nullptr, tb_b, 1.f, 0);
+    gb.j[0].Ssum = t_s; gb.j[0].Ssq = t_sq;
+    gemm_bf16<<<dim3(8, 16, 1), 256, 0, stream>>>(gb, 1024, 512, 512, -1, -1);
+  }
   {
     GemmBatch gb{};
-    gb.j[0] = {tb_b, w_ecWkg, nullptr, nullptr, nullptr, Kt_b, 1.f, 0};
-    gb.j[1] = {tb_b, w_ecWvg, nullptr, nullptr, nullptr, Vt_b, 1.f, 0};
-    gb.j[2] = {tb_b, w_pW, pb, nullptr, Et, nullptr, 1.f, 0};
-    gemm_bf16<<<dim3(8, 16, 3), 256, 0, stream>>>(gb, 1024, 512, 512);
-  }
-  mr_kernel<<<16384, 256, 0, stream>>>(dec_b, tb_b, md, q2d, mt, q2t, mArr,
-                                       rArr);
-  ec_attn<<<128, 256, 0, stream>>>(Qe_b, Kd_b, Kt_b, Vd_b, Vt_b, u_k, u_v, c_k,
-                                   c_v, mArr, rArr, Oec_b);
-  pool_kernel<<<dim3(64, 16), 256, 0, stream>>>(Ed, Et, pv, dec, tb_b, dec1);
+    gb.j[0] = J(tb_b, w_ecWkg, nullptr, nullptr, nullptr, Kt_b, 1.f, 0);
+    gb.j[1] = J(tb_b, w_ecWvg, nullptr, nullptr, nullptr, Vt_b, 1.f, 0);
+    gb.j[2] = J(tb_b, w_pW, pb, nullptr, Et, nullptr, 1.f, 0);
+    gb.mr = {dec_b, tb_b, md, q2d, t_s, t_sq, mArr, rArr};
+    gemm_bf16<<<dim3(8, 16, 4), 256, 0, stream>>>(gb, 1024, 512, 512, -1, 3);
+  }
+  attnpool<<<1152, 256, 0, stream>>>(Qe_b, Kd_b, Kt_b, Vd_b, Vt_b, u_k, u_v,
+                                     c_k, c_v, mArr, rArr, Oec_b, Ed, Et, pv,
+                                     dec, tb_b, dec1, d1s, d1q);
   {
     GemmBatch gb{};
-    gb.j[0] = {Oec_b, w_ecWo, ec_bo, enc, enc1, nullptr, 1.f, 0};
-    gemm_bf16<<<dim3(8, 16, 1), 256, 0, stream>>>(gb, 1024, 512, 512);
-  }
-  ln2_kernel<<<2048, 256, 0, stream>>>(enc1, n_es_g, n_es_b, nbE, dec1, n_ds_g,
-                                       n_ds_b, nbD);
+    gb.j[0] = J(Oec_b, w_ecWo, ec_bo, enc, enc1, nullptr, 1.f, 0);
+    gb.j[0].Ssum = e1s; gb.j[0].Ssq = e1q;
+    gemm_bf16<<<dim3(8, 16, 1), 256, 0, stream>>>(gb, 1024, 512, 512, -1, -1);
+  }
   {
     GemmBatch gb{};
-    gb.j[0] = {nbE, w_esWi, es_bi, nullptr, nullptr, QKVe_b, 1.f, 0};
-    gb.j[1] = {nbD, w_dsWi, ds_bi, nullptr, nullptr, QKVd_b, 1.f, 0};
-    gemm_bf16<<<dim3(24, 16, 2), 256, 0, stream>>>(gb, 1024, 1536, 512);
+    gb.j[0] = JF(enc1, e1s, e1q, n_es_g, n_es_b, w_esWi, es_bi, QKVe_b, 0);
+    gb.j[1] = JF(dec1, d1s, d1q, n_ds_g, n_ds_b, w_dsWi, ds_bi, QKVd_b, 0);
+    gemm_bf16<<<dim3(24, 16, 2), 256, 0, stream>>>(gb, 1024, 1536, 512, -1, -1);
   }
   self_attn<<<dim3(128, 2), 256, 0, stream>>>(QKVe_b, OaE, QKVd_b, OaD);
   {
     GemmBatch gb{};
-    gb.j[0] = {OaE, w_esWo, es_bo, enc1, enc2, nullptr, 1.f, 0};
-    gb.j[1] = {OaD, w_dsWo, ds_bo, dec1, dec2, nullptr, 1.f, 0};
-    gemm_bf16<<<dim3(8, 16, 2), 256, 0, stream>>>(gb, 1024, 512, 512);
-  }
-  ln2_kernel<<<2048, 256, 0, stream>>>(enc2, n_ef_g, n_ef_b, nbE, dec2, n_df_g,
-                                       n_df_b, nbD);
+    gb.j[0] = J(OaE, w_esWo, es_bo, enc1, enc2, nullptr, 1.f, 0);
+    gb.j[0].Ssum = e2s; gb.j[0].Ssq = e2q;
+    gb.j[1] = J(OaD, w_dsWo, ds_bo, dec1, dec2, nullptr, 1.f, 0);
+    gb.j[1].Ssum = d2s; gb.j[1].Ssq = d2q;
+    gemm_bf16<<<dim3(8, 16, 2), 256, 0, stream>>>(gb, 1024, 512, 512, -1, -1);
+  }
   {
     GemmBatch gb{};
-    gb.j[0] = {nbE, w_effW1, eff_b1, nullptr, nullptr, He_b, 1.f, 1};
-    gb.j[1] = {nbD, w_dffW1, dff_b1, nullptr, nullptr, Hd_b, 1.f, 1};
-    gemm_bf16<<<dim3(32, 16, 2), 256, 0, stream>>>(gb, 1024, 2048, 512);
+    gb.j[0] = JF(enc2, e2s, e2q, n_ef_g, n_ef_b, w_effW1, eff_b1, He_b, 1);
+    gb.j[1] = JF(dec2, d2s, d2q, n_df_g, n_df_b, w_dffW1, dff_b1, Hd_b, 1);
+    gemm_bf16<<<dim3(32, 16, 2), 256, 0, stream>>>(gb, 1024, 2048, 512, -1, -1);
   }
   float* out = (float*)d_out;
   {
     GemmBatch gb{};
-    gb.j[0] = {He_b, w_effW2, eff_b2, enc2, out, nullptr, 1.f, 0};
-    gb.j[1] = {Hd_b, w_dffW2, dff_b2, dec2, out + U, nullptr, 1.f, 0};
-    gemm_bf16<<<dim3(8, 16, 2), 256, 0, stream>>>(gb, 1024, 512, 2048);
-  }
-}
+    gb.j[0] = J(He_b, w_effW2, eff_b2, enc2, out, nullptr, 1.f, 0);
+    gb.j[1] = J(Hd_b, w_dffW2, dff_b2, dec2, out + U, nullptr, 1.f, 0);
+    gemm_bf16<<<dim3(8, 16, 2), 256, 0, stream>>>(gb, 1024, 512, 2048, -1, -1);
+  }
+}
```
